# Optimization experiments

Hardware: AMD Instinct MI355X
Metric: run time of the kernel (lower is better)

The kernel has to match this reference:

```python
import jax, jax.numpy as jnp
import numpy as np

H = 128
V = 50000
B = 128
T_C = 50
T_I = 32
T_Q = 32
EPISODES = 3


def gru_cell(x, h, Wih, Whh, bih, bhh):
    # torch GRUCell math
    gi = x @ Wih.T + bih
    gh = h @ Whh.T + bhh
    ir, iz, inn = jnp.split(gi, 3, axis=-1)
    hr, hz, hn = jnp.split(gh, 3, axis=-1)
    r = jax.nn.sigmoid(ir + hr)
    z = jax.nn.sigmoid(iz + hz)
    n = jnp.tanh(inn + r * hn)
    return (1.0 - z) * n + z * h


def gru_outputs(x, Wih, Whh, bih, bhh):
    # x: (N, T, H) -> hidden at every step, (N, T, H)
    h0 = jnp.zeros((x.shape[0], x.shape[2]), x.dtype)
    def step(h, xt):
        h2 = gru_cell(xt, h, Wih, Whh, bih, bhh)
        return h2, h2
    _, ys = jax.lax.scan(step, h0, jnp.swapaxes(x, 0, 1))
    return jnp.swapaxes(ys, 0, 1)


def setup_inputs():
    key = jax.random.key(0)
    ks = iter(jax.random.split(key, 48))
    s = 0.05
    def mat(shape):
        return (jax.random.normal(next(ks), shape) * s).astype(jnp.float32)
    def gru_p(in_dim):
        return mat((3 * H, in_dim)), mat((3 * H, H)), mat((3 * H,)), mat((3 * H,))
    embed = mat((V, H)).at[0].set(0.0)  # padding_idx=0
    ig_Wih, ig_Whh, ig_bih, ig_bhh = gru_p(H)
    qg_Wih, qg_Whh, qg_bih, qg_bhh = gru_p(H)
    at_Wih, at_Whh, at_bih, at_bhh = gru_p(H)
    me_Wih, me_Whh, me_bih, me_bhh = gru_p(H)
    an_Wih, an_Whh, an_bih, an_bhh = gru_p(2 * H)
    gate_W1 = mat((H, 4 * H)); gate_b1 = mat((H,))
    gate_W2 = mat((1, H)); gate_b2 = mat((1,))
    fc_W = mat((V, H)); fc_b = jnp.zeros((V,), jnp.float32)
    facts = jax.random.randint(next(ks), (B, T_C, T_I), 0, V)
    fact_masks = jnp.zeros((B, T_C, T_I), jnp.int32)  # 0 == real token
    questions = jax.random.randint(next(ks), (B, T_Q), 0, V)
    question_masks = jnp.zeros((B, T_Q), jnp.int32)
    return dict(facts=facts, fact_masks=fact_masks, questions=questions,
                question_masks=question_masks, num_decode=8, embed=embed,
                ig_Wih=ig_Wih, ig_Whh=ig_Whh, ig_bih=ig_bih, ig_bhh=ig_bhh,
                qg_Wih=qg_Wih, qg_Whh=qg_Whh, qg_bih=qg_bih, qg_bhh=qg_bhh,
                at_Wih=at_Wih, at_Whh=at_Whh, at_bih=at_bih, at_bhh=at_bhh,
                me_Wih=me_Wih, me_Whh=me_Whh, me_bih=me_bih, me_bhh=me_bhh,
                an_Wih=an_Wih, an_Whh=an_Whh, an_bih=an_bih, an_bhh=an_bhh,
                gate_W1=gate_W1, gate_b1=gate_b1, gate_W2=gate_W2, gate_b2=gate_b2,
                fc_W=fc_W, fc_b=fc_b)


def reference(facts, fact_masks, questions, question_masks, num_decode, embed,
              ig_Wih, ig_Whh, ig_bih, ig_bhh,
              qg_Wih, qg_Whh, qg_bih, qg_bhh,
              at_Wih, at_Whh, at_bih, at_bhh,
              me_Wih, me_Whh, me_bih, me_bhh,
              an_Wih, an_Whh, an_bih, an_bhh,
              gate_W1, gate_b1, gate_W2, gate_b2, fc_W, fc_b):
    Bv, Tc, Ti = facts.shape
    Hd = embed.shape[1]

    # ---- fact encoding: one batched GRU over all B*T_C facts ----
    f = facts.reshape(Bv * Tc, Ti)
    emb = embed[f]                                            # (B*Tc, Ti, H)
    outs = gru_outputs(emb, ig_Wih, ig_Whh, ig_bih, ig_bhh)
    flen = jnp.sum(fact_masks.reshape(Bv * Tc, Ti) == 0, axis=-1)
    enc_f = jnp.take_along_axis(outs, (flen - 1)[:, None, None], axis=1)[:, 0]
    enc_f = enc_f.reshape(Bv, Tc, Hd)                         # (B, T_C, H)

    # ---- question encoding ----
    qouts = gru_outputs(embed[questions], qg_Wih, qg_Whh, qg_bih, qg_bhh)
    qlen = jnp.sum(question_masks == 0, axis=-1)
    q = jnp.take_along_axis(qouts, (qlen - 1)[:, None, None], axis=1)[:, 0]  # (B, H)

    # ---- episodic memory ----
    memory = q
    facts_t = jnp.swapaxes(enc_f, 0, 1)                       # (T_C, B, H)
    for _ in range(EPISODES):
        m = memory
        def ep_step(h, ft):
            z = jnp.concatenate([ft * q, ft * m, jnp.abs(ft - q), jnp.abs(ft - m)], axis=-1)
            g = jax.nn.sigmoid(jnp.tanh(z @ gate_W1.T + gate_b1) @ gate_W2.T + gate_b2)  # (B,1)
            h2 = gru_cell(ft, h, at_Wih, at_Whh, at_bih, at_bhh)
            return g * h2 + (1.0 - g) * h, None
        e, _ = jax.lax.scan(ep_step, jnp.zeros_like(memory), facts_t)
        memory = gru_cell(e, memory, me_Wih, me_Whh, me_bih, me_bhh)

    # ---- answer decoding (y_{t-1} stays the <s> embedding, as in the source) ----
    y0 = jnp.broadcast_to(embed[2], (Bv, Hd))                 # <s> token id = 2
    yq = jnp.concatenate([y0, q], axis=-1)                    # (B, 2H)
    def dec_step(h, _):
        h2 = gru_cell(yq, h, an_Wih, an_Whh, an_bih, an_bhh)
        return h2, jax.nn.log_softmax(h2 @ fc_W.T + fc_b, axis=-1)
    _, dec = jax.lax.scan(dec_step, memory, None, length=num_decode)  # (T, B, V)
    return jnp.swapaxes(dec, 0, 1).reshape(Bv * num_decode, -1)
```

## Files before the change

### kernel.cpp

```cpp
#include <hip/hip_runtime.h>
#include <math.h>

#define H   128
#define H3  384
#define TC  50
#define TI  32
#define TQ  32
#define NB  128
#define NF  (NB*TC)
#define EPISODES 3

typedef short  bf16x8 __attribute__((ext_vector_type(8)));
typedef short  bf16x4 __attribute__((ext_vector_type(4)));
typedef float  f32x4  __attribute__((ext_vector_type(4)));

__device__ __forceinline__ float dot4(float4 a, float4 b) {
  return a.x*b.x + a.y*b.y + a.z*b.z + a.w*b.w;
}
__device__ __forceinline__ float sigm(float x) { return 1.f/(1.f + __expf(-x)); }
__device__ __forceinline__ float tanh_f(float x) { return 1.f - 2.f/(1.f + __expf(2.f*x)); }
__device__ __forceinline__ float gru_comb(float ir, float iz, float inn,
                                          float hr, float hz, float hn, float h) {
  float r = sigm(ir + hr);
  float z = sigm(iz + hz);
  float n = tanh_f(inn + r*hn);
  return (1.f - z)*n + z*h;
}
__device__ __forceinline__ short f2bf(float x) {
  union { float f; unsigned u; } v; v.f = x;
  unsigned r = v.u + 0x7fffu + ((v.u >> 16) & 1u);
  return (short)(r >> 16);
}
__device__ __forceinline__ float bf2f(short s) {
  union { unsigned u; float f; } v; v.u = ((unsigned)(unsigned short)s) << 16;
  return v.f;
}
__device__ __forceinline__ bf16x8 pack8(float4 lo, float4 hi) {
  bf16x8 o;
  o[0]=f2bf(lo.x); o[1]=f2bf(lo.y); o[2]=f2bf(lo.z); o[3]=f2bf(lo.w);
  o[4]=f2bf(hi.x); o[5]=f2bf(hi.y); o[6]=f2bf(hi.z); o[7]=f2bf(hi.w);
  return o;
}

__global__ __launch_bounds__(256) void k_cvtall(
    const float* __restrict__ emb, short* __restrict__ emb16,
    const float* __restrict__ fcw, short* __restrict__ fcw16,
    const float* __restrict__ w0, const float* __restrict__ w1,
    const float* __restrict__ w2, short* __restrict__ w16, int VH)
{
  int bid = blockIdx.x;
  const float* src; short* dst; int n, b0, nb;
  if (bid < 1280)      { src = emb; dst = emb16; n = VH; b0 = 0;    nb = 1280; }
  else if (bid < 2560) { src = fcw; dst = fcw16; n = VH; b0 = 1280; nb = 1280; }
  else {
    int j = (bid - 2560) / 24;
    src = (j == 0) ? w0 : ((j == 1) ? w1 : w2);
    dst = w16 + (size_t)j*H3*H;
    n = H3*H; b0 = 2560 + j*24; nb = 24;
  }
  int stride = nb*256*8;
  for (int i = ((bid - b0)*256 + threadIdx.x)*8; i < n; i += stride) {
    float4 lo = *(const float4*)(src + i);
    float4 hi = *(const float4*)(src + i + 4);
    *(bf16x8*)(dst + i) = pack8(lo, hi);
  }
}

__global__ __launch_bounds__(256) void k_gather16(const short* __restrict__ emb16,
    const int* __restrict__ toks, short* __restrict__ dst)
{
  int b0 = blockIdx.x * 8;
  int r = threadIdx.x >> 5, cc = (threadIdx.x & 31)*4;
  int t = toks[b0 + r];
  *(bf16x4*)(dst + (size_t)(b0 + r)*H + cc) = *(const bf16x4*)(emb16 + (size_t)t*H + cc);
}

__global__ __launch_bounds__(256) void k_mgemmX(const short* __restrict__ A16,
    const float* __restrict__ A32, const short* __restrict__ B16,
    const float* __restrict__ bias, short* __restrict__ C, int M, int N)
{
  __shared__ __align__(16) short As[64][136];
  __shared__ __align__(16) short Bs[128][136];
  int tid = threadIdx.x;
  int lane = tid & 63, wave = tid >> 6;
  int bm = blockIdx.x, bn = blockIdx.y;
  if (A16) {
    #pragma unroll
    for (int i = 0; i < 4; ++i) {
      int ch = tid + i*256;
      int r = ch >> 4, e = (ch & 15)*8;
      int gr = bm*64 + r; if (gr > M-1) gr = M-1;
      *(bf16x8*)&As[r][e] = *(const bf16x8*)(A16 + (size_t)gr*H + e);
    }
  } else {
    #pragma unroll
    for (int i = 0; i < 4; ++i) {
      int ch = tid + i*256;
      int r = ch >> 4, e = (ch & 15)*8;
      int gr = bm*64 + r; if (gr > M-1) gr = M-1;
      const float* src = A32 + (size_t)gr*H + e;
      *(bf16x8*)&As[r][e] = pack8(*(const float4*)src, *(const float4*)(src+4));
    }
  }
  #pragma unroll
  for (int i = 0; i < 8; ++i) {
    int ch = tid + i*256;
    int r = ch >> 4, e = (ch & 15)*8;
    int gn = bn*128 + r; if (gn > N-1) gn = N-1;
    *(bf16x8*)&Bs[r][e] = *(const bf16x8*)(B16 + (size_t)gn*H + e);
  }
  __syncthreads();
  int q = lane >> 4, l15 = lane & 15;
  f32x4 acc[8];
  #pragma unroll
  for (int nt = 0; nt < 8; ++nt) { acc[nt][0]=0.f; acc[nt][1]=0.f; acc[nt][2]=0.f; acc[nt][3]=0.f; }
  int mrow = wave*16 + l15;
  #pragma unroll
  for (int kf = 0; kf < 4; ++kf) {
    bf16x8 a = *(bf16x8*)&As[mrow][q*8 + kf*32];
    #pragma unroll
    for (int nt = 0; nt < 8; ++nt) {
      bf16x8 b = *(bf16x8*)&Bs[nt*16 + l15][q*8 + kf*32];
      acc[nt] = __builtin_amdgcn_mfma_f32_16x16x32_bf16(a, b, acc[nt], 0, 0, 0);
    }
  }
  __syncthreads();
  #pragma unroll
  for (int nt = 0; nt < 8; ++nt) {
    int col = nt*16 + l15;
    float bv = bias[bn*128 + col];
    #pragma unroll
    for (int reg = 0; reg < 4; ++reg)
      Bs[wave*16 + q*4 + reg][col] = f2bf(acc[nt][reg] + bv);
  }
  __syncthreads();
  #pragma unroll
  for (int i = 0; i < 4; ++i) {
    int idx = tid + i*256;
    int r = idx >> 4, e = (idx & 15)*8;
    int gr = bm*64 + r;
    if (gr < M) *(bf16x8*)(C + (size_t)gr*N + bn*128 + e) = *(bf16x8*)&Bs[r][e];
  }
}

#define GI_STR 392
__global__ __launch_bounds__(512) void k_recgru2(
    const short* __restrict__ GI, const int* __restrict__ masks,
    const float* __restrict__ Whh, const float* __restrict__ bhh,
    float* __restrict__ enc_out, float* __restrict__ mem_out, int steps)
{
  __shared__ __align__(16) short hsb[2][16][136];
  __shared__ __align__(16) short gib[2][16][GI_STR];
  __shared__ int enc_step_s[16];
  int tid = threadIdx.x;
  int lane = tid & 63, wave = tid >> 6;
  int q = lane >> 4, l15 = lane & 15;
  int seq0 = blockIdx.x * 16;

  for (int i = tid; i < 2*16*136; i += 512) ((short*)hsb)[i] = 0;
  if (tid < 16) {
    int fl = 0;
    for (int i = 0; i < steps; ++i) fl += (masks[(size_t)(seq0+tid)*steps + i] == 0);
    int et = fl - 1; if (et < 0) et = 0; if (et >= steps) et = steps-1;
    enc_step_s[tid] = et;
  }
  bf16x8 wfrag[3][4];
  #pragma unroll
  for (int i = 0; i < 3; ++i) {
    int n = 16*wave + 128*i + l15;
    const float* wr = Whh + (size_t)n*H + q*8;
    #pragma unroll
    for (int kf = 0; kf < 4; ++kf)
      wfrag[i][kf] = pack8(*(const float4*)(wr + kf*32), *(const float4*)(wr + kf*32 + 4));
  }
  int c = 16*wave + l15;
  float bh0 = bhh[c], bh1 = bhh[c+H], bh2 = bhh[c+2*H];
  int ch0 = tid, ch1 = tid + 512;
  int r0 = ch0/48, o0 = ch0 - r0*48;
  int r1 = ch1/48, o1 = ch1 - r1*48;
  __syncthreads();
  int es[4];
  #pragma unroll
  for (int reg = 0; reg < 4; ++reg) es[reg] = enc_step_s[q*4 + reg];

  {
    size_t row0 = (size_t)(seq0 + r0)*steps;
    *(bf16x8*)&gib[0][r0][o0*8] = *((const bf16x8*)(GI + row0*H3) + o0);
    if (tid < 256) {
      size_t row1 = (size_t)(seq0 + r1)*steps;
      *(bf16x8*)&gib[0][r1][o1*8] = *((const bf16x8*)(GI + row1*H3) + o1);
    }
  }
  __syncthreads();

  float hreg[4] = {0.f, 0.f, 0.f, 0.f};
  for (int t = 0; t < steps; ++t) {
    bf16x8 pf0, pf1;
    bool havepf = (t + 1 < steps);
    if (havepf) {
      size_t row0 = (size_t)(seq0 + r0)*steps + t + 1;
      pf0 = *((const bf16x8*)(GI + row0*H3) + o0);
      if (tid < 256) {
        size_t row1 = (size_t)(seq0 + r1)*steps + t + 1;
        pf1 = *((const bf16x8*)(GI + row1*H3) + o1);
      }
    }
    f32x4 acc[3];
    #pragma unroll
    for (int i = 0; i < 3; ++i) { acc[i][0]=0.f; acc[i][1]=0.f; acc[i][2]=0.f; acc[i][3]=0.f; }
    #pragma unroll
    for (int kf = 0; kf < 4; ++kf) {
      bf16x8 a = *(bf16x8*)&hsb[t & 1][l15][kf*32 + q*8];
      #pragma unroll
      for (int i = 0; i < 3; ++i)
        acc[i] = __builtin_amdgcn_mfma_f32_16x16x32_bf16(a, wfrag[i][kf], acc[i], 0, 0, 0);
    }
    #pragma unroll
    for (int reg = 0; reg < 4; ++reg) {
      int row = q*4 + reg;
      float gr = bf2f(gib[t & 1][row][c]);
      float gz = bf2f(gib[t & 1][row][c + 128]);
      float gn = bf2f(gib[t & 1][row][c + 256]);
      float hnew = gru_comb(gr, gz, gn,
                            acc[0][reg] + bh0, acc[1][reg] + bh1, acc[2][reg] + bh2,
                            hreg[reg]);
      hreg[reg] = hnew;
      hsb[(t + 1) & 1][row][c] = f2bf(hnew);
      if (t == es[reg]) {
        enc_out[(size_t)(seq0 + row)*H + c] = hnew;
        if (mem_out) mem_out[(size_t)(seq0 + row)*H + c] = hnew;
      }
    }
    if (havepf) {
      *(bf16x8*)&gib[(t + 1) & 1][r0][o0*8] = pf0;
      if (tid < 256) *(bf16x8*)&gib[(t + 1) & 1][r1][o1*8] = pf1;
    }
    __syncthreads();
  }
}

__global__ __launch_bounds__(512) void k_facts(
    const short* __restrict__ EMB16, const short* __restrict__ WI,
    const int* __restrict__ toks, const int* __restrict__ masks,
    const float* __restrict__ Whh, const float* __restrict__ bih,
    const float* __restrict__ bhh, float* __restrict__ enc_out, int steps)
{
  __shared__ __align__(16) short hsb[2][32][136];
  __shared__ __align__(16) short esb[2][32][136];
  __shared__ int ltoks[25*TI];
  __shared__ int enc_step_s[25];
  int tid = threadIdx.x;
  int lane = tid & 63, wave = tid >> 6;
  int q = lane >> 4, l15 = lane & 15;
  int seq0 = blockIdx.x * 25;

  for (int i = tid; i < 2*32*136; i += 512) { ((short*)hsb)[i] = 0; ((short*)esb)[i] = 0; }
  for (int i = tid; i < 25*steps; i += 512)
    ltoks[i] = toks[(size_t)seq0*steps + i];
  if (tid < 25) {
    int fl = 0;
    for (int i = 0; i < steps; ++i) fl += (masks[(size_t)(seq0+tid)*steps + i] == 0);
    int et = fl - 1; if (et < 0) et = 0; if (et >= steps) et = steps-1;
    enc_step_s[tid] = et;
  }
  bf16x8 wI[3][4], wH[3][4];
  #pragma unroll
  for (int i = 0; i < 3; ++i) {
    int n = 16*wave + 128*i + l15;
    #pragma unroll
    for (int kf = 0; kf < 4; ++kf) {
      wI[i][kf] = *(const bf16x8*)(WI + (size_t)n*H + kf*32 + q*8);
      const float* wr = Whh + (size_t)n*H + kf*32 + q*8;
      wH[i][kf] = pack8(*(const float4*)wr, *(const float4*)(wr + 4));
    }
  }
  int c = 16*wave + l15;
  float bi0 = bih[c], bi1 = bih[c+H], bi2 = bih[c+2*H];
  float bh0 = bhh[c], bh1 = bhh[c+H], bh2 = bhh[c+2*H];
  int er = tid >> 4, eo = tid & 15;
  bool act = er < 25;
  __syncthreads();
  int es0[4], es1[4];
  #pragma unroll
  for (int reg = 0; reg < 4; ++reg) {
    es0[reg] = enc_step_s[q*4 + reg];
    int row2 = 16 + q*4 + reg;
    es1[reg] = (row2 < 25) ? enc_step_s[row2] : -9;
  }
  if (act) {
    int tk = ltoks[er*steps];
    *(bf16x8*)&esb[0][er][eo*8] = *((const bf16x8*)(EMB16 + (size_t)tk*H) + eo);
  }
  __syncthreads();

  float h0[4] = {0.f,0.f,0.f,0.f}, h1[4] = {0.f,0.f,0.f,0.f};
  for (int t = 0; t < steps; ++t) {
    int cur = t & 1, nxt = cur ^ 1;
    bf16x8 pf;
    bool havepf = (t + 1 < steps) && act;
    if (havepf) {
      int tk = ltoks[er*steps + t + 1];
      pf = *((const bf16x8*)(EMB16 + (size_t)tk*H) + eo);
    }
    f32x4 gi[3], gh[3];
    gi[0] = (f32x4){bi0,bi0,bi0,bi0};
    gi[1] = (f32x4){bi1,bi1,bi1,bi1};
    gi[2] = (f32x4){bi2,bi2,bi2,bi2};
    gh[0] = (f32x4){bh0,bh0,bh0,bh0};
    gh[1] = (f32x4){bh1,bh1,bh1,bh1};
    gh[2] = (f32x4){bh2,bh2,bh2,bh2};
    #pragma unroll
    for (int kf = 0; kf < 4; ++kf) {
      bf16x8 ae = *(bf16x8*)&esb[cur][l15][kf*32 + q*8];
      bf16x8 ah = *(bf16x8*)&hsb[cur][l15][kf*32 + q*8];
      #pragma unroll
      for (int i = 0; i < 3; ++i) {
        gi[i] = __builtin_amdgcn_mfma_f32_16x16x32_bf16(ae, wI[i][kf], gi[i], 0, 0, 0);
        gh[i] = __builtin_amdgcn_mfma_f32_16x16x32_bf16(ah, wH[i][kf], gh[i], 0, 0, 0);
      }
    }
    #pragma unroll
    for (int reg = 0; reg < 4; ++reg) {
      int row = q*4 + reg;
      float hnew = gru_comb(gi[0][reg], gi[1][reg], gi[2][reg],
                            gh[0][reg], gh[1][reg], gh[2][reg], h0[reg]);
      h0[reg] = hnew;
      hsb[nxt][row][c] = f2bf(hnew);
      if (t == es0[reg]) enc_out[(size_t)(seq0 + row)*H + c] = hnew;
    }
    gi[0] = (f32x4){bi0,bi0,bi0,bi0};
    gi[1] = (f32x4){bi1,bi1,bi1,bi1};
    gi[2] = (f32x4){bi2,bi2,bi2,bi2};
    gh[0] = (f32x4){bh0,bh0,bh0,bh0};
    gh[1] = (f32x4){bh1,bh1,bh1,bh1};
    gh[2] = (f32x4){bh2,bh2,bh2,bh2};
    #pragma unroll
    for (int kf = 0; kf < 4; ++kf) {
      bf16x8 ae = *(bf16x8*)&esb[cur][16 + l15][kf*32 + q*8];
      bf16x8 ah = *(bf16x8*)&hsb[cur][16 + l15][kf*32 + q*8];
      #pragma unroll
      for (int i = 0; i < 3; ++i) {
        gi[i] = __builtin_amdgcn_mfma_f32_16x16x32_bf16(ae, wI[i][kf], gi[i], 0, 0, 0);
        gh[i] = __builtin_amdgcn_mfma_f32_16x16x32_bf16(ah, wH[i][kf], gh[i], 0, 0, 0);
      }
    }
    #pragma unroll
    for (int reg = 0; reg < 4; ++reg) {
      int row2 = 16 + q*4 + reg;
      if (row2 < 25) {
        float hnew = gru_comb(gi[0][reg], gi[1][reg], gi[2][reg],
                              gh[0][reg], gh[1][reg], gh[2][reg], h1[reg]);
        h1[reg] = hnew;
        hsb[nxt][row2][c] = f2bf(hnew);
        if (t == es1[reg]) enc_out[(size_t)(seq0 + row2)*H + c] = hnew;
      }
    }
    if (havepf) *(bf16x8*)&esb[nxt][er][eo*8] = pf;
    __syncthreads();
  }
}

__global__ __launch_bounds__(128) void k_gatepre2(const float* __restrict__ encf,
    const float* __restrict__ qv, const float* __restrict__ W1,
    const float* __restrict__ b1, const float* __restrict__ W2,
    const float* __restrict__ b2, float* __restrict__ U1, float* __restrict__ gate)
{
  __shared__ float us[16][H], vs[16][H], hid[16][H], parts[16][8];
  int tid = threadIdx.x;
  int nt0 = blockIdx.x * 16;
  for (int i = tid; i < 16*H; i += 128) {
    int r = i >> 7, k = i & 127;
    int nt = nt0 + r, n = nt / TC;
    float f = encf[(size_t)nt*H + k];
    float q = qv[(size_t)n*H + k];
    us[r][k] = f*q;
    vs[r][k] = fabsf(f - q);
  }
  __syncthreads();
  int c = tid;
  float acc[16] = {};
  {
    const float* wa = W1 + (size_t)c*(4*H);
    const float* wc = wa + 2*H;
    for (int kk = 0; kk < H; kk += 16) {
      float4 a0 = *(const float4*)(wa + kk);
      float4 a1 = *(const float4*)(wa + kk + 4);
      float4 a2 = *(const float4*)(wa + kk + 8);
      float4 a3 = *(const float4*)(wa + kk + 12);
      float4 c0 = *(const float4*)(wc + kk);
      float4 c1 = *(const float4*)(wc + kk + 4);
      float4 c2 = *(const float4*)(wc + kk + 8);
      float4 c3 = *(const float4*)(wc + kk + 12);
      #pragma unroll
      for (int r = 0; r < 16; ++r) {
        const float* up = &us[r][kk];
        const float* vp = &vs[r][kk];
        acc[r] += dot4(*(const float4*)up,     a0) + dot4(*(const float4*)(up+4), a1)
                + dot4(*(const float4*)(up+8), a2) + dot4(*(const float4*)(up+12),a3)
                + dot4(*(const float4*)vp,     c0) + dot4(*(const float4*)(vp+4), c1)
                + dot4(*(const float4*)(vp+8), c2) + dot4(*(const float4*)(vp+12),c3);
      }
    }
  }
  float accm[16] = {};
  {
    const float* wb = W1 + (size_t)c*(4*H) + H;
    const float* wd = W1 + (size_t)c*(4*H) + 3*H;
    for (int kk = 0; kk < H; kk += 16) {
      float4 a0 = *(const float4*)(wb + kk);
      float4 a1 = *(const float4*)(wb + kk + 4);
      float4 a2 = *(const float4*)(wb + kk + 8);
      float4 a3 = *(const float4*)(wb + kk + 12);
      float4 c0 = *(const float4*)(wd + kk);
      float4 c1 = *(const float4*)(wd + kk + 4);
      float4 c2 = *(const float4*)(wd + kk + 8);
      float4 c3 = *(const float4*)(wd + kk + 12);
      #pragma unroll
      for (int r = 0; r < 16; ++r) {
        const float* up = &us[r][kk];
        const float* vp = &vs[r][kk];
        accm[r] += dot4(*(const float4*)up,     a0) + dot4(*(const float4*)(up+4), a1)
                 + dot4(*(const float4*)(up+8), a2) + dot4(*(const float4*)(up+12),a3)
                 + dot4(*(const float4*)vp,     c0) + dot4(*(const float4*)(vp+4), c1)
                 + dot4(*(const float4*)(vp+8), c2) + dot4(*(const float4*)(vp+12),c3);
      }
    }
  }
  float bb = b1[c];
  #pragma unroll
  for (int r = 0; r < 16; ++r) {
    float u = acc[r] + bb;
    U1[(size_t)(nt0 + r)*H + c] = u;
    hid[r][c] = tanh_f(u + accm[r]);
  }
  __syncthreads();
  {
    int r = tid >> 3, i = tid & 7;
    float p = 0.f;
    for (int k = i*16; k < i*16 + 16; ++k) p += hid[r][k]*W2[k];
    parts[r][i] = p;
  }
  __syncthreads();
  if (tid < 16) {
    float s = b2[0];
    #pragma unroll
    for (int i = 0; i < 8; ++i) s += parts[tid][i];
    gate[nt0 + tid] = sigm(s);
  }
}

__global__ __launch_bounds__(128) void k_gate(const float* __restrict__ encf,
    const float* __restrict__ mem, const float* __restrict__ W1,
    const float* __restrict__ W2, const float* __restrict__ b2,
    const float* __restrict__ U1, float* __restrict__ gate)
{
  __shared__ float us[16][H], vs[16][H], hid[16][H], parts[16][8];
  int tid = threadIdx.x;
  int nt0 = blockIdx.x * 16;
  for (int i = tid; i < 16*H; i += 128) {
    int r = i >> 7, k = i & 127;
    int nt = nt0 + r, n = nt / TC;
    float f = encf[(size_t)nt*H + k];
    float m = mem[(size_t)n*H + k];
    us[r][k] = f*m;
    vs[r][k] = fabsf(f - m);
  }
  __syncthreads();
  int c = tid;
  float acc[16];
  #pragma unroll
  for (int r = 0; r < 16; ++r) acc[r] = U1[(size_t)(nt0 + r)*H + c];
  const float* wb = W1 + (size_t)c*(4*H) + H;
  const float* wd = W1 + (size_t)c*(4*H) + 3*H;
  for (int kk = 0; kk < H; kk += 16) {
    float4 a0 = *(const float4*)(wb + kk);
    float4 a1 = *(const float4*)(wb + kk + 4);
    float4 a2 = *(const float4*)(wb + kk + 8);
    float4 a3 = *(const float4*)(wb + kk + 12);
    float4 c0 = *(const float4*)(wd + kk);
    float4 c1 = *(const float4*)(wd + kk + 4);
    float4 c2 = *(const float4*)(wd + kk + 8);
    float4 c3 = *(const float4*)(wd + kk + 12);
    #pragma unroll
    for (int r = 0; r < 16; ++r) {
      const float* up = &us[r][kk];
      const float* vp = &vs[r][kk];
      acc[r] += dot4(*(const float4*)up,     a0) + dot4(*(const float4*)(up+4), a1)
              + dot4(*(const float4*)(up+8), a2) + dot4(*(const float4*)(up+12),a3)
              + dot4(*(const float4*)vp,     c0) + dot4(*(const float4*)(vp+4), c1)
              + dot4(*(const float4*)(vp+8), c2) + dot4(*(const float4*)(vp+12),c3);
    }
  }
  #pragma unroll
  for (int r = 0; r < 16; ++r) hid[r][c] = tanh_f(acc[r]);
  __syncthreads();
  {
    int r = tid >> 3, i = tid & 7;
    float p = 0.f;
    for (int k = i*16; k < i*16 + 16; ++k) p += hid[r][k]*W2[k];
    parts[r][i] = p;
  }
  __syncthreads();
  if (tid < 16) {
    float s = b2[0];
    #pragma unroll
    for (int i = 0; i < 8; ++i) s += parts[tid][i];
    gate[nt0 + tid] = sigm(s);
  }
}

__global__ __launch_bounds__(512) void k_episode2(
    const short* __restrict__ GIat, const float* __restrict__ gate,
    const float* __restrict__ at_Whh, const float* __restrict__ at_bhh,
    const float* __restrict__ me_Wih, const float* __restrict__ me_Whh,
    const float* __restrict__ me_bih, const float* __restrict__ me_bhh,
    float* __restrict__ mem)
{
  __shared__ __align__(16) short hsb[2][16][136];
  __shared__ __align__(16) short msb[16][136];
  __shared__ __align__(16) short gib[2][16][GI_STR];
  int tid = threadIdx.x;
  int lane = tid & 63, wave = tid >> 6;
  int q = lane >> 4, l15 = lane & 15;
  int n0 = blockIdx.x * 16;

  for (int i = tid; i < 2*16*136; i += 512) ((short*)hsb)[i] = 0;
  for (int i = tid; i < 16*H; i += 512) {
    int r = i >> 7, cc = i & 127;
    msb[r][cc] = f2bf(mem[(size_t)(n0 + r)*H + cc]);
  }
  bf16x8 wfrag[3][4];
  #pragma unroll
  for (int i = 0; i < 3; ++i) {
    int n = 16*wave + 128*i + l15;
    const float* wr = at_Whh + (size_t)n*H + q*8;
    #pragma unroll
    for (int kf = 0; kf < 4; ++kf)
      wfrag[i][kf] = pack8(*(const float4*)(wr + kf*32), *(const float4*)(wr + kf*32 + 4));
  }
  int c = 16*wave + l15;
  float bh0 = at_bhh[c], bh1 = at_bhh[c+H], bh2 = at_bhh[c+2*H];
  int ch0 = tid, ch1 = tid + 512;
  int r0 = ch0/48, o0 = ch0 - r0*48;
  int r1 = ch1/48, o1 = ch1 - r1*48;
  __syncthreads();

  *(bf16x8*)&gib[0][r0][o0*8] = *((const bf16x8*)(GIat + (size_t)(n0 + r0)*TC*H3) + o0);
  if (tid < 256)
    *(bf16x8*)&gib[0][r1][o1*8] = *((const bf16x8*)(GIat + (size_t)(n0 + r1)*TC*H3) + o1);
  __syncthreads();

  float hreg[4] = {0.f, 0.f, 0.f, 0.f};
  for (int t = 0; t < TC; ++t) {
    bf16x8 pf0, pf1;
    bool havepf = (t + 1 < TC);
    if (havepf) {
      pf0 = *((const bf16x8*)(GIat + ((size_t)(n0 + r0)*TC + t + 1)*H3) + o0);
      if (tid < 256)
        pf1 = *((const bf16x8*)(GIat + ((size_t)(n0 + r1)*TC + t + 1)*H3) + o1);
    }
    f32x4 acc[3];
    #pragma unroll
    for (int i = 0; i < 3; ++i) { acc[i][0]=0.f; acc[i][1]=0.f; acc[i][2]=0.f; acc[i][3]=0.f; }
    #pragma unroll
    for (int kf = 0; kf < 4; ++kf) {
      bf16x8 a = *(bf16x8*)&hsb[t & 1][l15][kf*32 + q*8];
      #pragma unroll
      for (int i = 0; i < 3; ++i)
        acc[i] = __builtin_amdgcn_mfma_f32_16x16x32_bf16(a, wfrag[i][kf], acc[i], 0, 0, 0);
    }
    #pragma unroll
    for (int reg = 0; reg < 4; ++reg) {
      int row = q*4 + reg;
      float g  = gate[(size_t)(n0 + row)*TC + t];
      float gr = bf2f(gib[t & 1][row][c]);
      float gz = bf2f(gib[t & 1][row][c + 128]);
      float gn = bf2f(gib[t & 1][row][c + 256]);
      float h2 = gru_comb(gr, gz, gn,
                          acc[0][reg] + bh0, acc[1][reg] + bh1, acc[2][reg] + bh2,
                          hreg[reg]);
      float hnew = g*h2 + (1.f - g)*hreg[reg];
      hreg[reg] = hnew;
      hsb[(t + 1) & 1][row][c] = f2bf(hnew);
    }
    if (havepf) {
      *(bf16x8*)&gib[(t + 1) & 1][r0][o0*8] = pf0;
      if (tid < 256) *(bf16x8*)&gib[(t + 1) & 1][r1][o1*8] = pf1;
    }
    __syncthreads();
  }
  f32x4 gi_acc[3], gh_acc[3];
  #pragma unroll
  for (int i = 0; i < 3; ++i) {
    gi_acc[i][0]=0.f; gi_acc[i][1]=0.f; gi_acc[i][2]=0.f; gi_acc[i][3]=0.f;
    gh_acc[i][0]=0.f; gh_acc[i][1]=0.f; gh_acc[i][2]=0.f; gh_acc[i][3]=0.f;
  }
  #pragma unroll
  for (int i = 0; i < 3; ++i) {
    int n = 16*wave + 128*i + l15;
    const float* wr = me_Wih + (size_t)n*H + q*8;
    #pragma unroll
    for (int kf = 0; kf < 4; ++kf)
      wfrag[i][kf] = pack8(*(const float4*)(wr + kf*32), *(const float4*)(wr + kf*32 + 4));
  }
  #pragma unroll
  for (int kf = 0; kf < 4; ++kf) {
    bf16x8 a = *(bf16x8*)&hsb[TC & 1][l15][kf*32 + q*8];
    #pragma unroll
    for (int i = 0; i < 3; ++i)
      gi_acc[i] = __builtin_amdgcn_mfma_f32_16x16x32_bf16(a, wfrag[i][kf], gi_acc[i], 0, 0, 0);
  }
  #pragma unroll
  for (int i = 0; i < 3; ++i) {
    int n = 16*wave + 128*i + l15;
    const float* wr = me_Whh + (size_t)n*H + q*8;
    #pragma unroll
    for (int kf = 0; kf < 4; ++kf)
      wfrag[i][kf] = pack8(*(const float4*)(wr + kf*32), *(const float4*)(wr + kf*32 + 4));
  }
  #pragma unroll
  for (int kf = 0; kf < 4; ++kf) {
    bf16x8 a = *(bf16x8*)&msb[l15][kf*32 + q*8];
    #pragma unroll
    for (int i = 0; i < 3; ++i)
      gh_acc[i] = __builtin_amdgcn_mfma_f32_16x16x32_bf16(a, wfrag[i][kf], gh_acc[i], 0, 0, 0);
  }
  float bi0 = me_bih[c], bi1 = me_bih[c+H], bi2 = me_bih[c+2*H];
  float bo0 = me_bhh[c], bo1 = me_bhh[c+H], bo2 = me_bhh[c+2*H];
  #pragma unroll
  for (int reg = 0; reg < 4; ++reg) {
    int row = q*4 + reg;
    float m = mem[(size_t)(n0 + row)*H + c];
    float mnew = gru_comb(gi_acc[0][reg] + bi0, gi_acc[1][reg] + bi1, gi_acc[2][reg] + bi2,
                          gh_acc[0][reg] + bo0, gh_acc[1][reg] + bo1, gh_acc[2][reg] + bo2, m);
    mem[(size_t)(n0 + row)*H + c] = mnew;
  }
}

__global__ __launch_bounds__(384) void k_decode(const float* __restrict__ embed,
    const float* __restrict__ qv, const float* __restrict__ mem,
    const float* __restrict__ an_Wih, const float* __restrict__ an_Whh,
    const float* __restrict__ an_bih, const float* __restrict__ an_bhh,
    short* __restrict__ h2d16, int ND)
{
  __shared__ float hs[2][H], qs[2][H], e2[H], ghs[2][H3], gis[2][H3];
  int tid = threadIdx.x;
  int n0 = blockIdx.x * 2;
  if (tid < H) e2[tid] = embed[2*H + tid];
  if (tid < 256) {
    int r = tid >> 7, c = tid & 127;
    hs[r][c] = mem[(size_t)(n0 + r)*H + c];
    qs[r][c] = qv[(size_t)(n0 + r)*H + c];
  }
  __syncthreads();
  {
    const float* wp = an_Wih + (size_t)tid*(2*H);
    float se = 0.f, sq0 = 0.f, sq1 = 0.f;
    for (int kk = 0; kk < H; kk += 16) {
      float4 w0 = *(const float4*)(wp + kk);
      float4 w1 = *(const float4*)(wp + kk + 4);
      float4 w2 = *(const float4*)(wp + kk + 8);
      float4 w3 = *(const float4*)(wp + kk + 12);
      const float* ep = &e2[kk];
      se += dot4(*(const float4*)ep,     w0) + dot4(*(const float4*)(ep+4), w1)
          + dot4(*(const float4*)(ep+8), w2) + dot4(*(const float4*)(ep+12),w3);
      float4 u0 = *(const float4*)(wp + H + kk);
      float4 u1 = *(const float4*)(wp + H + kk + 4);
      float4 u2 = *(const float4*)(wp + H + kk + 8);
      float4 u3 = *(const float4*)(wp + H + kk + 12);
      const float* q0 = &qs[0][kk];
      const float* q1 = &qs[1][kk];
      sq0 += dot4(*(const float4*)q0,     u0) + dot4(*(const float4*)(q0+4), u1)
           + dot4(*(const float4*)(q0+8), u2) + dot4(*(const float4*)(q0+12),u3);
      sq1 += dot4(*(const float4*)q1,     u0) + dot4(*(const float4*)(q1+4), u1)
           + dot4(*(const float4*)(q1+8), u2) + dot4(*(const float4*)(q1+12),u3);
    }
    float b = an_bih[tid];
    gis[0][tid] = b + se + sq0;
    gis[1][tid] = b + se + sq1;
  }
  const float* whp = an_Whh + (size_t)tid*H;
  float bh = an_bhh[tid];
  for (int t = 0; t < ND; ++t) {
    float a0 = 0.f, a1 = 0.f;
    for (int kk = 0; kk < H; kk += 16) {
      float4 w0 = *(const float4*)(whp + kk);
      float4 w1 = *(const float4*)(whp + kk + 4);
      float4 w2 = *(const float4*)(whp + kk + 8);
      float4 w3 = *(const float4*)(whp + kk + 12);
      const float* h0p = &hs[0][kk];
      const float* h1p = &hs[1][kk];
      a0 += dot4(*(const float4*)h0p,     w0) + dot4(*(const float4*)(h0p+4), w1)
          + dot4(*(const float4*)(h0p+8), w2) + dot4(*(const float4*)(h0p+12),w3);
      a1 += dot4(*(const float4*)h1p,     w0) + dot4(*(const float4*)(h1p+4), w1)
          + dot4(*(const float4*)(h1p+8), w2) + dot4(*(const float4*)(h1p+12),w3);
    }
    ghs[0][tid] = a0 + bh;
    ghs[1][tid] = a1 + bh;
    __syncthreads();
    if (tid < 256) {
      int r = tid >> 7, c = tid & 127;
      float h2 = gru_comb(gis[r][c], gis[r][c+H], gis[r][c+2*H],
                          ghs[r][c], ghs[r][c+H], ghs[r][c+2*H], hs[r][c]);
      hs[r][c] = h2;
      h2d16[((size_t)(n0 + r)*ND + t)*H + c] = f2bf(h2);
    }
    __syncthreads();
  }
}

__global__ __launch_bounds__(256) void k_lpass1p(const short* __restrict__ A16,
    const short* __restrict__ B16, const float* __restrict__ bias,
    float2* __restrict__ partials, int M, int N, int NSL)
{
  __shared__ __align__(16) short As[64][136];
  __shared__ __align__(16) short Bs[128][136];
  int tid = threadIdx.x;
  int lane = tid & 63, wave = tid >> 6;
  int q = lane >> 4, l15 = lane & 15;
  int bn = blockIdx.x;
  #pragma unroll
  for (int i = 0; i < 8; ++i) {
    int ch = tid + i*256;
    int r = ch >> 4, e = (ch & 15)*8;
    int gn = bn*128 + r; if (gn > N-1) gn = N-1;
    *(bf16x8*)&Bs[r][e] = *(const bf16x8*)(B16 + (size_t)gn*H + e);
  }
  float bv[8];
  #pragma unroll
  for (int nt = 0; nt < 8; ++nt) {
    int col = bn*128 + nt*16 + l15;
    bv[nt] = (col < N) ? bias[col] : 0.f;
  }
  int mrow = wave*16 + l15;
  for (int rt = 0; rt < 16; ++rt) {
    __syncthreads();
    #pragma unroll
    for (int i = 0; i < 4; ++i) {
      int ch = tid + i*256;
      int r = ch >> 4, e = (ch & 15)*8;
      *(bf16x8*)&As[r][e] = *(const bf16x8*)(A16 + (size_t)(rt*64 + r)*H + e);
    }
    __syncthreads();
    f32x4 acc[8];
    #pragma unroll
    for (int nt = 0; nt < 8; ++nt) { acc[nt][0]=0.f; acc[nt][1]=0.f; acc[nt][2]=0.f; acc[nt][3]=0.f; }
    #pragma unroll
    for (int kf = 0; kf < 4; ++kf) {
      bf16x8 a = *(bf16x8*)&As[mrow][q*8 + kf*32];
      #pragma unroll
      for (int nt = 0; nt < 8; ++nt) {
        bf16x8 b = *(bf16x8*)&Bs[nt*16 + l15][q*8 + kf*32];
        acc[nt] = __builtin_amdgcn_mfma_f32_16x16x32_bf16(a, b, acc[nt], 0, 0, 0);
      }
    }
    #pragma unroll
    for (int reg = 0; reg < 4; ++reg) {
      float xs[8], cm = -3.4e38f;
      #pragma unroll
      for (int nt = 0; nt < 8; ++nt) {
        int col = bn*128 + nt*16 + l15;
        float x = (col < N) ? (acc[nt][reg] + bv[nt]) : -3.4e38f;
        xs[nt] = x; cm = fmaxf(cm, x);
      }
      #pragma unroll
      for (int off = 1; off < 16; off <<= 1) cm = fmaxf(cm, __shfl_xor(cm, off));
      float ss = 0.f;
      #pragma unroll
      for (int nt = 0; nt < 8; ++nt) ss += __expf(xs[nt] - cm);
      #pragma unroll
      for (int off = 1; off < 16; off <<= 1) ss += __shfl_xor(ss, off);
      if (l15 == 0) {
        int row = rt*64 + wave*16 + q*4 + reg;
        partials[(size_t)row*NSL + bn] = make_float2(cm, ss);
      }
    }
  }
}

__global__ __launch_bounds__(256) void k_lse2(const float2* __restrict__ partials,
                                              float* __restrict__ lse, int M, int NSL)
{
  int wave = threadIdx.x >> 6, lane = threadIdx.x & 63;
  int row = blockIdx.x*4 + wave;
  if (row >= M) return;
  float m = -3.4e38f, s = 0.f;
  for (int i = lane; i < NSL; i += 64) {
    float2 p = partials[(size_t)row*NSL + i];
    float nm = fmaxf(m, p.x);
    s = s*__expf(m - nm) + p.y*__expf(p.x - nm);
    m = nm;
  }
  #pragma unroll
  for (int off = 32; off; off >>= 1) {
    float mo = __shfl_xor(m, off);
    float so = __shfl_xor(s, off);
    float nm = fmaxf(m, mo);
    s = s*__expf(m - nm) + so*__expf(mo - nm);
    m = nm;
  }
  if (lane == 0) lse[row] = m + logf(s);
}

__global__ __launch_bounds__(256) void k_lpass2p(const short* __restrict__ A16,
    const short* __restrict__ B16, const float* __restrict__ bias,
    const float* __restrict__ lse, float* __restrict__ C, int M, int N, int NT)
{
  __shared__ __align__(16) short As[64][136];
  __shared__ __align__(16) short Bs[128][136];
  __shared__ float lss[960];
  int tid = threadIdx.x;
  int lane = tid & 63, wave = tid >> 6;
  int q = lane >> 4, l15 = lane & 15;
  int bn = blockIdx.x;
  #pragma unroll
  for (int i = 0; i < 8; ++i) {
    int ch = tid + i*256;
    int r = ch >> 4, e = (ch & 15)*8;
    int gn = bn*128 + r; if (gn > N-1) gn = N-1;
    *(bf16x8*)&Bs[r][e] = *(const bf16x8*)(B16 + (size_t)gn*H + e);
  }
  for (int i = tid; i < NT*64; i += 256) lss[i] = lse[i];
  float bv[8];
  #pragma unroll
  for (int nt = 0; nt < 8; ++nt) {
    int col = bn*128 + nt*16 + l15;
    bv[nt] = (col < N) ? bias[col] : 0.f;
  }
  int mrow = wave*16 + l15;
  for (int rt = 0; rt < NT; ++rt) {
    __syncthreads();
    #pragma unroll
    for (int i = 0; i < 4; ++i) {
      int ch = tid + i*256;
      int r = ch >> 4, e = (ch & 15)*8;
      *(bf16x8*)&As[r][e] = *(const bf16x8*)(A16 + (size_t)(rt*64 + r)*H + e);
    }
    __syncthreads();
    f32x4 acc[8];
    #pragma unroll
    for (int nt = 0; nt < 8; ++nt) { acc[nt][0]=0.f; acc[nt][1]=0.f; acc[nt][2]=0.f; acc[nt][3]=0.f; }
    #pragma unroll
    for (int kf = 0; kf < 4; ++kf) {
      bf16x8 a = *(bf16x8*)&As[mrow][q*8 + kf*32];
      #pragma unroll
      for (int nt = 0; nt < 8; ++nt) {
        bf16x8 b = *(bf16x8*)&Bs[nt*16 + l15][q*8 + kf*32];
        acc[nt] = __builtin_amdgcn_mfma_f32_16x16x32_bf16(a, b, acc[nt], 0, 0, 0);
      }
    }
    #pragma unroll
    for (int nt = 0; nt < 8; ++nt) {
      int gcol = bn*128 + nt*16 + l15;
      if (gcol < N) {
        #pragma unroll
        for (int reg = 0; reg < 4; ++reg) {
          int row = rt*64 + wave*16 + q*4 + reg;
          C[(size_t)row*N + gcol] = acc[nt][reg] + bv[nt] - lss[row];
        }
      }
    }
  }
}

__global__ __launch_bounds__(256) void k_lpass2(const short* __restrict__ A16,
    const short* __restrict__ B16, const float* __restrict__ B32,
    const float* __restrict__ bias, const float* __restrict__ lse,
    float* __restrict__ C, int M, int N, int bm_off)
{
  __shared__ __align__(16) short As[64][136];
  __shared__ __align__(16) short Bs[128][136];
  int tid = threadIdx.x;
  int lane = tid & 63, wave = tid >> 6;
  int q = lane >> 4, l15 = lane & 15;
  int bm = blockIdx.x + bm_off, bn = blockIdx.y;
  #pragma unroll
  for (int i = 0; i < 4; ++i) {
    int ch = tid + i*256;
    int r = ch >> 4, e = (ch & 15)*8;
    int gr = bm*64 + r; if (gr > M-1) gr = M-1;
    *(bf16x8*)&As[r][e] = *(const bf16x8*)(A16 + (size_t)gr*H + e);
  }
  if (B16) {
    #pragma unroll
    for (int i = 0; i < 8; ++i) {
      int ch = tid + i*256;
      int r = ch >> 4, e = (ch & 15)*8;
      int gn = bn*128 + r; if (gn > N-1) gn = N-1;
      *(bf16x8*)&Bs[r][e] = *(const bf16x8*)(B16 + (size_t)gn*H + e);
    }
  } else {
    #pragma unroll
    for (int i = 0; i < 8; ++i) {
      int ch = tid + i*256;
      int r = ch >> 4, e = (ch & 15)*8;
      int gn = bn*128 + r; if (gn > N-1) gn = N-1;
      const float* src = B32 + (size_t)gn*H + e;
      *(bf16x8*)&Bs[r][e] = pack8(*(const float4*)src, *(const float4*)(src+4));
    }
  }
  __syncthreads();
  f32x4 acc[8];
  #pragma unroll
  for (int nt = 0; nt < 8; ++nt) { acc[nt][0]=0.f; acc[nt][1]=0.f; acc[nt][2]=0.f; acc[nt][3]=0.f; }
  int mrow = wave*16 + l15;
  #pragma unroll
  for (int kf = 0; kf < 4; ++kf) {
    bf16x8 a = *(bf16x8*)&As[mrow][q*8 + kf*32];
    #pragma unroll
    for (int nt = 0; nt < 8; ++nt) {
      bf16x8 b = *(bf16x8*)&Bs[nt*16 + l15][q*8 + kf*32];
      acc[nt] = __builtin_amdgcn_mfma_f32_16x16x32_bf16(a, b, acc[nt], 0, 0, 0);
    }
  }
  __syncthreads();
  float (*Cs)[132] = (float(*)[132])&Bs[0][0];
  float lrow[4];
  #pragma unroll
  for (int reg = 0; reg < 4; ++reg) {
    int row = bm*64 + wave*16 + q*4 + reg;
    lrow[reg] = lse[row < M ? row : M-1];
  }
  #pragma unroll
  for (int nt = 0; nt < 8; ++nt) {
    int col = nt*16 + l15;
    int gcol = bn*128 + col;
    float bv = (gcol < N) ? bias[gcol] : 0.f;
    #pragma unroll
    for (int reg = 0; reg < 4; ++reg)
      Cs[wave*16 + q*4 + reg][col] = acc[nt][reg] + bv - lrow[reg];
  }
  __syncthreads();
  #pragma unroll
  for (int i = 0; i < 8; ++i) {
    int idx = tid + i*256;
    int r = idx >> 5, c4 = (idx & 31)*4;
    int gr = bm*64 + r;
    int gc = bn*128 + c4;
    if (gr < M && gc + 3 < N)
      *(float4*)(C + (size_t)gr*N + gc) = *(float4*)&Cs[r][c4];
    else if (gr < M) {
      #pragma unroll
      for (int j = 0; j < 4; ++j)
        if (gc + j < N) C[(size_t)gr*N + gc + j] = Cs[r][c4 + j];
    }
  }
}

extern "C" void kernel_launch(void* const* d_in, const int* in_sizes, int n_in,
                              void* d_out, int out_size, void* d_ws, size_t ws_size,
                              hipStream_t stream) {
  const int*   facts     = (const int*)  d_in[0];
  const int*   fmask     = (const int*)  d_in[1];
  const int*   questions = (const int*)  d_in[2];
  const int*   qmask     = (const int*)  d_in[3];
  const float* embed     = (const float*)d_in[5];
  const float* ig_Wih    = (const float*)d_in[6];
  const float* ig_Whh    = (const float*)d_in[7];
  const float* ig_bih    = (const float*)d_in[8];
  const float* ig_bhh    = (const float*)d_in[9];
  const float* qg_Wih    = (const float*)d_in[10];
  const float* qg_Whh    = (const float*)d_in[11];
  const float* qg_bih    = (const float*)d_in[12];
  const float* qg_bhh    = (const float*)d_in[13];
  const float* at_Wih    = (const float*)d_in[14];
  const float* at_Whh    = (const float*)d_in[15];
  const float* at_bih    = (const float*)d_in[16];
  const float* at_bhh    = (const float*)d_in[17];
  const float* me_Wih    = (const float*)d_in[18];
  const float* me_Whh    = (const float*)d_in[19];
  const float* me_bih    = (const float*)d_in[20];
  const float* me_bhh    = (const float*)d_in[21];
  const float* an_Wih    = (const float*)d_in[22];
  const float* an_Whh    = (const float*)d_in[23];
  const float* an_bih    = (const float*)d_in[24];
  const float* an_bhh    = (const float*)d_in[25];
  const float* gate_W1   = (const float*)d_in[26];
  const float* gate_b1   = (const float*)d_in[27];
  const float* gate_W2   = (const float*)d_in[28];
  const float* gate_b2   = (const float*)d_in[29];
  const float* fc_W      = (const float*)d_in[30];
  const float* fc_b      = (const float*)d_in[31];
  (void)n_in; (void)ws_size;

  const int V   = in_sizes[5] / H;
  const int ND  = out_size / (NB * V);
  const int M   = NB * ND;
  const int NSL = (V + 127) / 128;

  float* OUT = (float*)d_out;
  size_t oPART  = 0;
  size_t oEMB16 = oPART + (size_t)M*NSL*2;
  size_t oEMBQ  = oEMB16 + (size_t)V*64;
  size_t oQGI   = oEMBQ + (size_t)NB*TQ*64;
  size_t oGIAT  = oQGI  + (size_t)NB*TQ*192;
  size_t oU1    = oGIAT + (size_t)NF*192;
  size_t oGATE  = oU1   + (size_t)NF*H;
  size_t oW16   = oGATE + NF;
  float2* partials = (float2*)(OUT + oPART);
  short* EMB16  = (short*)(OUT + oEMB16);
  short* EMBQ16 = (short*)(OUT + oEMBQ);
  short* QGIsh  = (short*)(OUT + oQGI);
  short* GIATsh = (short*)(OUT + oGIAT);
  float* U1b    = OUT + oU1;
  float* GATE   = OUT + oGATE;
  short* igW16  = (short*)(OUT + oW16);
  short* qgW16  = igW16 + (size_t)H3*H;
  short* atW16  = qgW16 + (size_t)H3*H;
  short* FCW16  = (short*)(OUT + (size_t)(M - 64)*V);

  float* encf  = (float*)d_ws;
  float* qvec  = encf + (size_t)NF*H;
  float* mem   = qvec + (size_t)NB*H;
  short* H2D16 = (short*)(mem + (size_t)NB*H);
  float* lse   = (float*)(H2D16 + (size_t)M*H);

  k_cvtall<<<2632, 256, 0, stream>>>(embed, EMB16, fc_W, FCW16,
                                     ig_Wih, qg_Wih, at_Wih, igW16, V*H);
  k_gather16<<<NB*TQ/8, 256, 0, stream>>>(EMB16, questions, EMBQ16);
  k_mgemmX<<<dim3(NB*TQ/64, H3/128), 256, 0, stream>>>(EMBQ16, nullptr, qgW16, qg_bih, QGIsh, NB*TQ, H3);
  k_facts<<<NF/25, 512, 0, stream>>>(EMB16, igW16, facts, fmask, ig_Whh, ig_bih, ig_bhh, encf, TI);
  k_recgru2<<<NB/16, 512, 0, stream>>>(QGIsh, qmask, qg_Whh, qg_bhh, qvec, mem, TQ);
  k_mgemmX<<<dim3(NF/64, H3/128), 256, 0, stream>>>(nullptr, encf, atW16, at_bih, GIATsh, NF, H3);
  k_gatepre2<<<NF/16, 128, 0, stream>>>(encf, qvec, gate_W1, gate_b1, gate_W2, gate_b2, U1b, GATE);
  k_episode2<<<NB/16, 512, 0, stream>>>(GIATsh, GATE, at_Whh, at_bhh,
                                        me_Wih, me_Whh, me_bih, me_bhh, mem);
  for (int e = 1; e < EPISODES; ++e) {
    k_gate<<<NF/16, 128, 0, stream>>>(encf, mem, gate_W1, gate_W2, gate_b2, U1b, GATE);
    k_episode2<<<NB/16, 512, 0, stream>>>(GIATsh, GATE, at_Whh, at_bhh,
                                          me_Wih, me_Whh, me_bih, me_bhh, mem);
  }
  k_decode<<<NB/2, 384, 0, stream>>>(embed, qvec, mem, an_Wih, an_Whh, an_bih, an_bhh,
                                     H2D16, ND);
  k_lpass1p<<<NSL, 256, 0, stream>>>(H2D16, FCW16, fc_b, partials, M, V, NSL);
  k_lse2<<<(M+3)/4, 256, 0, stream>>>(partials, lse, M, NSL);
  k_lpass2p<<<NSL, 256, 0, stream>>>(H2D16, FCW16, fc_b, lse, OUT, M, V, (M/64) - 1);
  k_lpass2<<<dim3(1, NSL), 256, 0, stream>>>(H2D16, nullptr, fc_W, fc_b, lse,
                                             OUT, M, V, (M/64) - 1);
}
```

Baseline: 956.7 us.

## Fuse question gather, facts/question GRUs, GIAT gemm with gate, coalesce logits stores

```diff
diff --git a/kernel.cpp b/kernel.cpp
--- a/kernel.cpp
+++ b/kernel.cpp
@@ -66,17 +66,8 @@
   }
 }
 
-__global__ __launch_bounds__(256) void k_gather16(const short* __restrict__ emb16,
-    const int* __restrict__ toks, short* __restrict__ dst)
-{
-  int b0 = blockIdx.x * 8;
-  int r = threadIdx.x >> 5, cc = (threadIdx.x & 31)*4;
-  int t = toks[b0 + r];
-  *(bf16x4*)(dst + (size_t)(b0 + r)*H + cc) = *(const bf16x4*)(emb16 + (size_t)t*H + cc);
-}
-
 __global__ __launch_bounds__(256) void k_mgemmX(const short* __restrict__ A16,
-    const float* __restrict__ A32, const short* __restrict__ B16,
+    const int* __restrict__ toks, const short* __restrict__ B16,
     const float* __restrict__ bias, short* __restrict__ C, int M, int N)
 {
   __shared__ __align__(16) short As[64][136];
@@ -84,23 +75,13 @@
   int tid = threadIdx.x;
   int lane = tid & 63, wave = tid >> 6;
   int bm = blockIdx.x, bn = blockIdx.y;
-  if (A16) {
-    #pragma unroll
-    for (int i = 0; i < 4; ++i) {
-      int ch = tid + i*256;
-      int r = ch >> 4, e = (ch & 15)*8;
-      int gr = bm*64 + r; if (gr > M-1) gr = M-1;
-      *(bf16x8*)&As[r][e] = *(const bf16x8*)(A16 + (size_t)gr*H + e);
-    }
-  } else {
-    #pragma unroll
-    for (int i = 0; i < 4; ++i) {
-      int ch = tid + i*256;
-      int r = ch >> 4, e = (ch & 15)*8;
-      int gr = bm*64 + r; if (gr > M-1) gr = M-1;
-      const float* src = A32 + (size_t)gr*H + e;
-      *(bf16x8*)&As[r][e] = pack8(*(const float4*)src, *(const float4*)(src+4));
-    }
+  #pragma unroll
+  for (int i = 0; i < 4; ++i) {
+    int ch = tid + i*256;
+    int r = ch >> 4, e = (ch & 15)*8;
+    int gr = bm*64 + r; if (gr > M-1) gr = M-1;
+    size_t arow = toks ? (size_t)toks[gr] : (size_t)gr;
+    *(bf16x8*)&As[r][e] = *(const bf16x8*)(A16 + arow*H + e);
   }
   #pragma unroll
   for (int i = 0; i < 8; ++i) {
@@ -144,320 +125,388 @@
 }
 
 #define GI_STR 392
-__global__ __launch_bounds__(512) void k_recgru2(
-    const short* __restrict__ GI, const int* __restrict__ masks,
-    const float* __restrict__ Whh, const float* __restrict__ bhh,
-    float* __restrict__ enc_out, float* __restrict__ mem_out, int steps)
+__global__ __launch_bounds__(512) void k_factsq(
+    const short* __restrict__ EMB16, const short* __restrict__ WI,
+    const int* __restrict__ toks, const int* __restrict__ masks,
+    const float* __restrict__ Whh, const float* __restrict__ bih,
+    const float* __restrict__ bhh, float* __restrict__ enc_out,
+    const short* __restrict__ QGI, const int* __restrict__ qmasks,
+    const float* __restrict__ qWhh, const float* __restrict__ qbhh,
+    float* __restrict__ qvec, float* __restrict__ mem_out)
 {
-  __shared__ __align__(16) short hsb[2][16][136];
-  __shared__ __align__(16) short gib[2][16][GI_STR];
-  __shared__ int enc_step_s[16];
+  __shared__ __align__(16) char smem[38464];
   int tid = threadIdx.x;
   int lane = tid & 63, wave = tid >> 6;
   int q = lane >> 4, l15 = lane & 15;
-  int seq0 = blockIdx.x * 16;
-
-  for (int i = tid; i < 2*16*136; i += 512) ((short*)hsb)[i] = 0;
-  if (tid < 16) {
-    int fl = 0;
-    for (int i = 0; i < steps; ++i) fl += (masks[(size_t)(seq0+tid)*steps + i] == 0);
-    int et = fl - 1; if (et < 0) et = 0; if (et >= steps) et = steps-1;
-    enc_step_s[tid] = et;
-  }
-  bf16x8 wfrag[3][4];
-  #pragma unroll
-  for (int i = 0; i < 3; ++i) {
-    int n = 16*wave + 128*i + l15;
-    const float* wr = Whh + (size_t)n*H + q*8;
-    #pragma unroll
-    for (int kf = 0; kf < 4; ++kf)
-      wfrag[i][kf] = pack8(*(const float4*)(wr + kf*32), *(const float4*)(wr + kf*32 + 4));
-  }
-  int c = 16*wave + l15;
-  float bh0 = bhh[c], bh1 = bhh[c+H], bh2 = bhh[c+2*H];
-  int ch0 = tid, ch1 = tid + 512;
-  int r0 = ch0/48, o0 = ch0 - r0*48;
-  int r1 = ch1/48, o1 = ch1 - r1*48;
-  __syncthreads();
-  int es[4];
-  #pragma unroll
-  for (int reg = 0; reg < 4; ++reg) es[reg] = enc_step_s[q*4 + reg];
-
-  {
-    size_t row0 = (size_t)(seq0 + r0)*steps;
-    *(bf16x8*)&gib[0][r0][o0*8] = *((const bf16x8*)(GI + row0*H3) + o0);
-    if (tid < 256) {
-      size_t row1 = (size_t)(seq0 + r1)*steps;
-      *(bf16x8*)&gib[0][r1][o1*8] = *((const bf16x8*)(GI + row1*H3) + o1);
-    }
-  }
-  __syncthreads();
-
-  float hreg[4] = {0.f, 0.f, 0.f, 0.f};
-  for (int t = 0; t < steps; ++t) {
-    bf16x8 pf0, pf1;
-    bool havepf = (t + 1 < steps);
-    if (havepf) {
-      size_t row0 = (size_t)(seq0 + r0)*steps + t + 1;
-      pf0 = *((const bf16x8*)(GI + row0*H3) + o0);
+
+  if (blockIdx.x < 256) {
+    short (*hsb)[136] = (short(*)[136])smem;
+    short (*esb)[136] = (short(*)[136])(smem + 17408);
+    int* ltoks = (int*)(smem + 34816);
+    int* enc_step_s = (int*)(smem + 38016);
+    int seq0 = blockIdx.x * 25;
+    const int steps = TI;
+
+    {
+      short* p0 = (short*)smem;
+      short* p1 = (short*)(smem + 17408);
+      for (int i = tid; i < 2*32*136; i += 512) { p0[i] = 0; p1[i] = 0; }
+    }
+    for (int i = tid; i < 25*steps; i += 512)
+      ltoks[i] = toks[(size_t)seq0*steps + i];
+    if (tid < 25) {
+      int fl = 0;
+      for (int i = 0; i < steps; ++i) fl += (masks[(size_t)(seq0+tid)*steps + i] == 0);
+      int et = fl - 1; if (et < 0) et = 0; if (et >= steps) et = steps-1;
+      enc_step_s[tid] = et;
+    }
+    bf16x8 wI[3][4], wH[3][4];
+    #pragma unroll
+    for (int i = 0; i < 3; ++i) {
+      int n = 16*wave + 128*i + l15;
+      #pragma unroll
+      for (int kf = 0; kf < 4; ++kf) {
+        wI[i][kf] = *(const bf16x8*)(WI + (size_t)n*H + kf*32 + q*8);
+        const float* wr = Whh + (size_t)n*H + kf*32 + q*8;
+        wH[i][kf] = pack8(*(const float4*)wr, *(const float4*)(wr + 4));
+      }
+    }
+    int c = 16*wave + l15;
+    float bi0 = bih[c], bi1 = bih[c+H], bi2 = bih[c+2*H];
+    float bh0 = bhh[c], bh1 = bhh[c+H], bh2 = bhh[c+2*H];
+    int er = tid >> 4, eo = tid & 15;
+    bool act = er < 25;
+    __syncthreads();
+    int es0[4], es1[4];
+    #pragma unroll
+    for (int reg = 0; reg < 4; ++reg) {
+      es0[reg] = enc_step_s[q*4 + reg];
+      int row2 = 16 + q*4 + reg;
+      es1[reg] = (row2 < 25) ? enc_step_s[row2] : -9;
+    }
+    if (act) {
+      int tk = ltoks[er*steps];
+      *(bf16x8*)&esb[er][eo*8] = *((const bf16x8*)(EMB16 + (size_t)tk*H) + eo);
+    }
+    __syncthreads();
+
+    float h0[4] = {0.f,0.f,0.f,0.f}, h1[4] = {0.f,0.f,0.f,0.f};
+    for (int t = 0; t < steps; ++t) {
+      int cur = (t & 1)*32, nxt = ((t+1) & 1)*32;
+      bf16x8 pf;
+      bool havepf = (t + 1 < steps) && act;
+      if (havepf) {
+        int tk = ltoks[er*steps + t + 1];
+        pf = *((const bf16x8*)(EMB16 + (size_t)tk*H) + eo);
+      }
+      f32x4 gi[3], gh[3];
+      gi[0] = (f32x4){bi0,bi0,bi0,bi0};
+      gi[1] = (f32x4){bi1,bi1,bi1,bi1};
+      gi[2] = (f32x4){bi2,bi2,bi2,bi2};
+      gh[0] = (f32x4){bh0,bh0,bh0,bh0};
+      gh[1] = (f32x4){bh1,bh1,bh1,bh1};
+      gh[2] = (f32x4){bh2,bh2,bh2,bh2};
+      #pragma unroll
+      for (int kf = 0; kf < 4; ++kf) {
+        bf16x8 ae = *(bf16x8*)&esb[cur + l15][kf*32 + q*8];
+        bf16x8 ah = *(bf16x8*)&hsb[cur + l15][kf*32 + q*8];
+        #pragma unroll
+        for (int i = 0; i < 3; ++i) {
+          gi[i] = __builtin_amdgcn_mfma_f32_16x16x32_bf16(ae, wI[i][kf], gi[i], 0, 0, 0);
+          gh[i] = __builtin_amdgcn_mfma_f32_16x16x32_bf16(ah, wH[i][kf], gh[i], 0, 0, 0);
+        }
+      }
+      #pragma unroll
+      for (int reg = 0; reg < 4; ++reg) {
+        int row = q*4 + reg;
+        float hnew = gru_comb(gi[0][reg], gi[1][reg], gi[2][reg],
+                              gh[0][reg], gh[1][reg], gh[2][reg], h0[reg]);
+        h0[reg] = hnew;
+        hsb[nxt + row][c] = f2bf(hnew);
+        if (t == es0[reg]) enc_out[(size_t)(seq0 + row)*H + c] = hnew;
+      }
+      gi[0] = (f32x4){bi0,bi0,bi0,bi0};
+      gi[1] = (f32x4){bi1,bi1,bi1,bi1};
+      gi[2] = (f32x4){bi2,bi2,bi2,bi2};
+      gh[0] = (f32x4){bh0,bh0,bh0,bh0};
+      gh[1] = (f32x4){bh1,bh1,bh1,bh1};
+      gh[2] = (f32x4){bh2,bh2,bh2,bh2};
+      #pragma unroll
+      for (int kf = 0; kf < 4; ++kf) {
+        bf16x8 ae = *(bf16x8*)&esb[cur + 16 + l15][kf*32 + q*8];
+        bf16x8 ah = *(bf16x8*)&hsb[cur + 16 + l15][kf*32 + q*8];
+        #pragma unroll
+        for (int i = 0; i < 3; ++i) {
+          gi[i] = __builtin_amdgcn_mfma_f32_16x16x32_bf16(ae, wI[i][kf], gi[i], 0, 0, 0);
+          gh[i] = __builtin_amdgcn_mfma_f32_16x16x32_bf16(ah, wH[i][kf], gh[i], 0, 0, 0);
+        }
+      }
+      #pragma unroll
+      for (int reg = 0; reg < 4; ++reg) {
+        int row2 = 16 + q*4 + reg;
+        if (row2 < 25) {
+          float hnew = gru_comb(gi[0][reg], gi[1][reg], gi[2][reg],
+                                gh[0][reg], gh[1][reg], gh[2][reg], h1[reg]);
+          h1[reg] = hnew;
+          hsb[nxt + row2][c] = f2bf(hnew);
+          if (t == es1[reg]) enc_out[(size_t)(seq0 + row2)*H + c] = hnew;
+        }
+      }
+      if (havepf) *(bf16x8*)&esb[nxt + er][eo*8] = pf;
+      __syncthreads();
+    }
+  } else {
+    short (*hsb)[136] = (short(*)[136])smem;
+    short (*gib)[GI_STR] = (short(*)[GI_STR])(smem + 8704);
+    int* enc_step_s = (int*)(smem + 33792);
+    int seq0 = (blockIdx.x - 256) * 16;
+    const int steps = TQ;
+
+    {
+      short* p0 = (short*)smem;
+      for (int i = tid; i < 2*16*136; i += 512) p0[i] = 0;
+    }
+    if (tid < 16) {
+      int fl = 0;
+      for (int i = 0; i < steps; ++i) fl += (qmasks[(size_t)(seq0+tid)*steps + i] == 0);
+      int et = fl - 1; if (et < 0) et = 0; if (et >= steps) et = steps-1;
+      enc_step_s[tid] = et;
+    }
+    bf16x8 wfrag[3][4];
+    #pragma unroll
+    for (int i = 0; i < 3; ++i) {
+      int n = 16*wave + 128*i + l15;
+      const float* wr = qWhh + (size_t)n*H + q*8;
+      #pragma unroll
+      for (int kf = 0; kf < 4; ++kf)
+        wfrag[i][kf] = pack8(*(const float4*)(wr + kf*32), *(const float4*)(wr + kf*32 + 4));
+    }
+    int c = 16*wave + l15;
+    float bh0 = qbhh[c], bh1 = qbhh[c+H], bh2 = qbhh[c+2*H];
+    int ch0 = tid, ch1 = tid + 512;
+    int r0 = ch0/48, o0 = ch0 - r0*48;
+    int r1 = ch1/48, o1 = ch1 - r1*48;
+    __syncthreads();
+    int es[4];
+    #pragma unroll
+    for (int reg = 0; reg < 4; ++reg) es[reg] = enc_step_s[q*4 + reg];
+
+    {
+      size_t row0 = (size_t)(seq0 + r0)*steps;
+      *(bf16x8*)&gib[r0][o0*8] = *((const bf16x8*)(QGI + row0*H3) + o0);
       if (tid < 256) {
-        size_t row1 = (size_t)(seq0 + r1)*steps + t + 1;
-        pf1 = *((const bf16x8*)(GI + row1*H3) + o1);
-      }
-    }
-    f32x4 acc[3];
-    #pragma unroll
-    for (int i = 0; i < 3; ++i) { acc[i][0]=0.f; acc[i][1]=0.f; acc[i][2]=0.f; acc[i][3]=0.f; }
-    #pragma unroll
-    for (int kf = 0; kf < 4; ++kf) {
-      bf16x8 a = *(bf16x8*)&hsb[t & 1][l15][kf*32 + q*8];
-      #pragma unroll
-      for (int i = 0; i < 3; ++i)
-        acc[i] = __builtin_amdgcn_mfma_f32_16x16x32_bf16(a, wfrag[i][kf], acc[i], 0, 0, 0);
-    }
-    #pragma unroll
-    for (int reg = 0; reg < 4; ++reg) {
-      int row = q*4 + reg;
-      float gr = bf2f(gib[t & 1][row][c]);
-      float gz = bf2f(gib[t & 1][row][c + 128]);
-      float gn = bf2f(gib[t & 1][row][c + 256]);
-      float hnew = gru_comb(gr, gz, gn,
-                            acc[0][reg] + bh0, acc[1][reg] + bh1, acc[2][reg] + bh2,
-                            hreg[reg]);
-      hreg[reg] = hnew;
-      hsb[(t + 1) & 1][row][c] = f2bf(hnew);
-      if (t == es[reg]) {
-        enc_out[(size_t)(seq0 + row)*H + c] = hnew;
-        if (mem_out) mem_out[(size_t)(seq0 + row)*H + c] = hnew;
-      }
-    }
-    if (havepf) {
-      *(bf16x8*)&gib[(t + 1) & 1][r0][o0*8] = pf0;
-      if (tid < 256) *(bf16x8*)&gib[(t + 1) & 1][r1][o1*8] = pf1;
-    }
-    __syncthreads();
-  }
-}
-
-__global__ __launch_bounds__(512) void k_facts(
-    const short* __restrict__ EMB16, const short* __restrict__ WI,
-    const int* __restrict__ toks, const int* __restrict__ masks,
-    const float* __restrict__ Whh, const float* __restrict__ bih,
-    const float* __restrict__ bhh, float* __restrict__ enc_out, int steps)
-{
-  __shared__ __align__(16) short hsb[2][32][136];
-  __shared__ __align__(16) short esb[2][32][136];
-  __shared__ int ltoks[25*TI];
-  __shared__ int enc_step_s[25];
-  int tid = threadIdx.x;
-  int lane = tid & 63, wave = tid >> 6;
-  int q = lane >> 4, l15 = lane & 15;
-  int seq0 = blockIdx.x * 25;
-
-  for (int i = tid; i < 2*32*136; i += 512) { ((short*)hsb)[i] = 0; ((short*)esb)[i] = 0; }
-  for (int i = tid; i < 25*steps; i += 512)
-    ltoks[i] = toks[(size_t)seq0*steps + i];
-  if (tid < 25) {
-    int fl = 0;
-    for (int i = 0; i < steps; ++i) fl += (masks[(size_t)(seq0+tid)*steps + i] == 0);
-    int et = fl - 1; if (et < 0) et = 0; if (et >= steps) et = steps-1;
-    enc_step_s[tid] = et;
-  }
-  bf16x8 wI[3][4], wH[3][4];
-  #pragma unroll
-  for (int i = 0; i < 3; ++i) {
-    int n = 16*wave + 128*i + l15;
-    #pragma unroll
-    for (int kf = 0; kf < 4; ++kf) {
-      wI[i][kf] = *(const bf16x8*)(WI + (size_t)n*H + kf*32 + q*8);
-      const float* wr = Whh + (size_t)n*H + kf*32 + q*8;
-      wH[i][kf] = pack8(*(const float4*)wr, *(const float4*)(wr + 4));
-    }
-  }
-  int c = 16*wave + l15;
-  float bi0 = bih[c], bi1 = bih[c+H], bi2 = bih[c+2*H];
-  float bh0 = bhh[c], bh1 = bhh[c+H], bh2 = bhh[c+2*H];
-  int er = tid >> 4, eo = tid & 15;
-  bool act = er < 25;
-  __syncthreads();
-  int es0[4], es1[4];
-  #pragma unroll
-  for (int reg = 0; reg < 4; ++reg) {
-    es0[reg] = enc_step_s[q*4 + reg];
-    int row2 = 16 + q*4 + reg;
-    es1[reg] = (row2 < 25) ? enc_step_s[row2] : -9;
-  }
-  if (act) {
-    int tk = ltoks[er*steps];
-    *(bf16x8*)&esb[0][er][eo*8] = *((const bf16x8*)(EMB16 + (size_t)tk*H) + eo);
-  }
-  __syncthreads();
-
-  float h0[4] = {0.f,0.f,0.f,0.f}, h1[4] = {0.f,0.f,0.f,0.f};
-  for (int t = 0; t < steps; ++t) {
-    int cur = t & 1, nxt = cur ^ 1;
-    bf16x8 pf;
-    bool havepf = (t + 1 < steps) && act;
-    if (havepf) {
-      int tk = ltoks[er*steps + t + 1];
-      pf = *((const bf16x8*)(EMB16 + (size_t)tk*H) + eo);
-    }
-    f32x4 gi[3], gh[3];
-    gi[0] = (f32x4){bi0,bi0,bi0,bi0};
-    gi[1] = (f32x4){bi1,bi1,bi1,bi1};
-    gi[2] = (f32x4){bi2,bi2,bi2,bi2};
-    gh[0] = (f32x4){bh0,bh0,bh0,bh0};
-    gh[1] = (f32x4){bh1,bh1,bh1,bh1};
-    gh[2] = (f32x4){bh2,bh2,bh2,bh2};
-    #pragma unroll
-    for (int kf = 0; kf < 4; ++kf) {
-      bf16x8 ae = *(bf16x8*)&esb[cur][l15][kf*32 + q*8];
-      bf16x8 ah = *(bf16x8*)&hsb[cur][l15][kf*32 + q*8];
-      #pragma unroll
-      for (int i = 0; i < 3; ++i) {
-        gi[i] = __builtin_amdgcn_mfma_f32_16x16x32_bf16(ae, wI[i][kf], gi[i], 0, 0, 0);
-        gh[i] = __builtin_amdgcn_mfma_f32_16x16x32_bf16(ah, wH[i][kf], gh[i], 0, 0, 0);
-      }
-    }
-    #pragma unroll
-    for (int reg = 0; reg < 4; ++reg) {
-      int row = q*4 + reg;
-      float hnew = gru_comb(gi[0][reg], gi[1][reg], gi[2][reg],
-                            gh[0][reg], gh[1][reg], gh[2][reg], h0[reg]);
-      h0[reg] = hnew;
-      hsb[nxt][row][c] = f2bf(hnew);
-      if (t == es0[reg]) enc_out[(size_t)(seq0 + row)*H + c] = hnew;
-    }
-    gi[0] = (f32x4){bi0,bi0,bi0,bi0};
-    gi[1] = (f32x4){bi1,bi1,bi1,bi1};
-    gi[2] = (f32x4){bi2,bi2,bi2,bi2};
-    gh[0] = (f32x4){bh0,bh0,bh0,bh0};
-    gh[1] = (f32x4){bh1,bh1,bh1,bh1};
-    gh[2] = (f32x4){bh2,bh2,bh2,bh2};
-    #pragma unroll
-    for (int kf = 0; kf < 4; ++kf) {
-      bf16x8 ae = *(bf16x8*)&esb[cur][16 + l15][kf*32 + q*8];
-      bf16x8 ah = *(bf16x8*)&hsb[cur][16 + l15][kf*32 + q*8];
-      #pragma unroll
-      for (int i = 0; i < 3; ++i) {
-        gi[i] = __builtin_amdgcn_mfma_f32_16x16x32_bf16(ae, wI[i][kf], gi[i], 0, 0, 0);
-        gh[i] = __builtin_amdgcn_mfma_f32_16x16x32_bf16(ah, wH[i][kf], gh[i], 0, 0, 0);
-      }
-    }
-    #pragma unroll
-    for (int reg = 0; reg < 4; ++reg) {
-      int row2 = 16 + q*4 + reg;
-      if (row2 < 25) {
-        float hnew = gru_comb(gi[0][reg], gi[1][reg], gi[2][reg],
-                              gh[0][reg], gh[1][reg], gh[2][reg], h1[reg]);
-        h1[reg] = hnew;
-        hsb[nxt][row2][c] = f2bf(hnew);
-        if (t == es1[reg]) enc_out[(size_t)(seq0 + row2)*H + c] = hnew;
-      }
-    }
-    if (havepf) *(bf16x8*)&esb[nxt][er][eo*8] = pf;
-    __syncthreads();
-  }
-}
-
-__global__ __launch_bounds__(128) void k_gatepre2(const float* __restrict__ encf,
+        size_t row1 = (size_t)(seq0 + r1)*steps;
+        *(bf16x8*)&gib[r1][o1*8] = *((const bf16x8*)(QGI + row1*H3) + o1);
+      }
+    }
+    __syncthreads();
+
+    float hreg[4] = {0.f, 0.f, 0.f, 0.f};
+    for (int t = 0; t < steps; ++t) {
+      int cur = (t & 1)*16, nxt = ((t+1) & 1)*16;
+      bf16x8 pf0, pf1;
+      bool havepf = (t + 1 < steps);
+      if (havepf) {
+        size_t row0 = (size_t)(seq0 + r0)*steps + t + 1;
+        pf0 = *((const bf16x8*)(QGI + row0*H3) + o0);
+        if (tid < 256) {
+          size_t row1 = (size_t)(seq0 + r1)*steps + t + 1;
+          pf1 = *((const bf16x8*)(QGI + row1*H3) + o1);
+        }
+      }
+      f32x4 acc[3];
+      #pragma unroll
+      for (int i = 0; i < 3; ++i) { acc[i][0]=0.f; acc[i][1]=0.f; acc[i][2]=0.f; acc[i][3]=0.f; }
+      #pragma unroll
+      for (int kf = 0; kf < 4; ++kf) {
+        bf16x8 a = *(bf16x8*)&hsb[cur + l15][kf*32 + q*8];
+        #pragma unroll
+        for (int i = 0; i < 3; ++i)
+          acc[i] = __builtin_amdgcn_mfma_f32_16x16x32_bf16(a, wfrag[i][kf], acc[i], 0, 0, 0);
+      }
+      #pragma unroll
+      for (int reg = 0; reg < 4; ++reg) {
+        int row = q*4 + reg;
+        float gr = bf2f(gib[cur + row][c]);
+        float gz = bf2f(gib[cur + row][c + 128]);
+        float gn = bf2f(gib[cur + row][c + 256]);
+        float hnew = gru_comb(gr, gz, gn,
+                              acc[0][reg] + bh0, acc[1][reg] + bh1, acc[2][reg] + bh2,
+                              hreg[reg]);
+        hreg[reg] = hnew;
+        hsb[nxt + row][c] = f2bf(hnew);
+        if (t == es[reg]) {
+          qvec[(size_t)(seq0 + row)*H + c] = hnew;
+          mem_out[(size_t)(seq0 + row)*H + c] = hnew;
+        }
+      }
+      if (havepf) {
+        *(bf16x8*)&gib[nxt + r0][o0*8] = pf0;
+        if (tid < 256) *(bf16x8*)&gib[nxt + r1][o1*8] = pf1;
+      }
+      __syncthreads();
+    }
+  }
+}
+
+__global__ __launch_bounds__(256) void k_giat_gate0(
+    const float* __restrict__ encf, const short* __restrict__ atW16,
+    const float* __restrict__ at_bih, short* __restrict__ GIAT,
     const float* __restrict__ qv, const float* __restrict__ W1,
     const float* __restrict__ b1, const float* __restrict__ W2,
     const float* __restrict__ b2, float* __restrict__ U1, float* __restrict__ gate)
 {
-  __shared__ float us[16][H], vs[16][H], hid[16][H], parts[16][8];
+  __shared__ __align__(16) char smem[52224];
   int tid = threadIdx.x;
-  int nt0 = blockIdx.x * 16;
-  for (int i = tid; i < 16*H; i += 128) {
-    int r = i >> 7, k = i & 127;
-    int nt = nt0 + r, n = nt / TC;
-    float f = encf[(size_t)nt*H + k];
-    float q = qv[(size_t)n*H + k];
-    us[r][k] = f*q;
-    vs[r][k] = fabsf(f - q);
-  }
-  __syncthreads();
-  int c = tid;
-  float acc[16] = {};
-  {
-    const float* wa = W1 + (size_t)c*(4*H);
-    const float* wc = wa + 2*H;
-    for (int kk = 0; kk < H; kk += 16) {
-      float4 a0 = *(const float4*)(wa + kk);
-      float4 a1 = *(const float4*)(wa + kk + 4);
-      float4 a2 = *(const float4*)(wa + kk + 8);
-      float4 a3 = *(const float4*)(wa + kk + 12);
-      float4 c0 = *(const float4*)(wc + kk);
-      float4 c1 = *(const float4*)(wc + kk + 4);
-      float4 c2 = *(const float4*)(wc + kk + 8);
-      float4 c3 = *(const float4*)(wc + kk + 12);
-      #pragma unroll
-      for (int r = 0; r < 16; ++r) {
-        const float* up = &us[r][kk];
-        const float* vp = &vs[r][kk];
-        acc[r] += dot4(*(const float4*)up,     a0) + dot4(*(const float4*)(up+4), a1)
-                + dot4(*(const float4*)(up+8), a2) + dot4(*(const float4*)(up+12),a3)
-                + dot4(*(const float4*)vp,     c0) + dot4(*(const float4*)(vp+4), c1)
-                + dot4(*(const float4*)(vp+8), c2) + dot4(*(const float4*)(vp+12),c3);
-      }
-    }
-  }
-  float accm[16] = {};
-  {
-    const float* wb = W1 + (size_t)c*(4*H) + H;
-    const float* wd = W1 + (size_t)c*(4*H) + 3*H;
-    for (int kk = 0; kk < H; kk += 16) {
-      float4 a0 = *(const float4*)(wb + kk);
-      float4 a1 = *(const float4*)(wb + kk + 4);
-      float4 a2 = *(const float4*)(wb + kk + 8);
-      float4 a3 = *(const float4*)(wb + kk + 12);
-      float4 c0 = *(const float4*)(wd + kk);
-      float4 c1 = *(const float4*)(wd + kk + 4);
-      float4 c2 = *(const float4*)(wd + kk + 8);
-      float4 c3 = *(const float4*)(wd + kk + 12);
-      #pragma unroll
-      for (int r = 0; r < 16; ++r) {
-        const float* up = &us[r][kk];
-        const float* vp = &vs[r][kk];
-        accm[r] += dot4(*(const float4*)up,     a0) + dot4(*(const float4*)(up+4), a1)
-                 + dot4(*(const float4*)(up+8), a2) + dot4(*(const float4*)(up+12),a3)
-                 + dot4(*(const float4*)vp,     c0) + dot4(*(const float4*)(vp+4), c1)
-                 + dot4(*(const float4*)(vp+8), c2) + dot4(*(const float4*)(vp+12),c3);
-      }
-    }
-  }
-  float bb = b1[c];
-  #pragma unroll
-  for (int r = 0; r < 16; ++r) {
-    float u = acc[r] + bb;
-    U1[(size_t)(nt0 + r)*H + c] = u;
-    hid[r][c] = tanh_f(u + accm[r]);
-  }
-  __syncthreads();
-  {
-    int r = tid >> 3, i = tid & 7;
-    float p = 0.f;
-    for (int k = i*16; k < i*16 + 16; ++k) p += hid[r][k]*W2[k];
-    parts[r][i] = p;
-  }
-  __syncthreads();
-  if (tid < 16) {
-    float s = b2[0];
-    #pragma unroll
-    for (int i = 0; i < 8; ++i) s += parts[tid][i];
-    gate[nt0 + tid] = sigm(s);
-  }
-}
-
-__global__ __launch_bounds__(128) void k_gate(const float* __restrict__ encf,
+  if (blockIdx.x < 300) {
+    short (*As)[136] = (short(*)[136])smem;
+    short (*Bs)[136] = (short(*)[136])(smem + 17408);
+    int bm = blockIdx.x % 100, bn = blockIdx.x / 100;
+    int lane = tid & 63, wave = tid >> 6;
+    int q = lane >> 4, l15 = lane & 15;
+    #pragma unroll
+    for (int i = 0; i < 4; ++i) {
+      int ch = tid + i*256;
+      int r = ch >> 4, e = (ch & 15)*8;
+      int gr = bm*64 + r;
+      const float* src = encf + (size_t)gr*H + e;
+      *(bf16x8*)&As[r][e] = pack8(*(const float4*)src, *(const float4*)(src+4));
+    }
+    #pragma unroll
+    for (int i = 0; i < 8; ++i) {
+      int ch = tid + i*256;
+      int r = ch >> 4, e = (ch & 15)*8;
+      int gn = bn*128 + r;
+      *(bf16x8*)&Bs[r][e] = *(const bf16x8*)(atW16 + (size_t)gn*H + e);
+    }
+    __syncthreads();
+    f32x4 acc[8];
+    #pragma unroll
+    for (int nt = 0; nt < 8; ++nt) { acc[nt][0]=0.f; acc[nt][1]=0.f; acc[nt][2]=0.f; acc[nt][3]=0.f; }
+    int mrow = wave*16 + l15;
+    #pragma unroll
+    for (int kf = 0; kf < 4; ++kf) {
+      bf16x8 a = *(bf16x8*)&As[mrow][q*8 + kf*32];
+      #pragma unroll
+      for (int nt = 0; nt < 8; ++nt) {
+        bf16x8 b = *(bf16x8*)&Bs[nt*16 + l15][q*8 + kf*32];
+        acc[nt] = __builtin_amdgcn_mfma_f32_16x16x32_bf16(a, b, acc[nt], 0, 0, 0);
+      }
+    }
+    __syncthreads();
+    #pragma unroll
+    for (int nt = 0; nt < 8; ++nt) {
+      int col = nt*16 + l15;
+      float bv = at_bih[bn*128 + col];
+      #pragma unroll
+      for (int reg = 0; reg < 4; ++reg)
+        Bs[wave*16 + q*4 + reg][col] = f2bf(acc[nt][reg] + bv);
+    }
+    __syncthreads();
+    #pragma unroll
+    for (int i = 0; i < 4; ++i) {
+      int idx = tid + i*256;
+      int r = idx >> 4, e = (idx & 15)*8;
+      int gr = bm*64 + r;
+      *(bf16x8*)(GIAT + (size_t)gr*H3 + bn*128 + e) = *(bf16x8*)&Bs[r][e];
+    }
+  } else {
+    float* us = (float*)smem;
+    float* vs = us + 32*128;
+    float* hid = vs + 32*128;
+    float* parts = hid + 32*128;
+    int nt0 = (blockIdx.x - 300) * 32;
+    for (int i = tid; i < 32*128; i += 256) {
+      int r = i >> 7, k = i & 127;
+      int nt = nt0 + r, n = nt / TC;
+      float f = encf[(size_t)nt*H + k];
+      float qq = qv[(size_t)n*H + k];
+      us[i] = f*qq;
+      vs[i] = fabsf(f - qq);
+    }
+    __syncthreads();
+    int c = tid & 127, rbase = (tid >> 7)*16;
+    float acc[16] = {};
+    {
+      const float* wa = W1 + (size_t)c*(4*H);
+      const float* wc = wa + 2*H;
+      for (int kk = 0; kk < H; kk += 16) {
+        float4 a0 = *(const float4*)(wa + kk);
+        float4 a1 = *(const float4*)(wa + kk + 4);
+        float4 a2 = *(const float4*)(wa + kk + 8);
+        float4 a3 = *(const float4*)(wa + kk + 12);
+        float4 c0 = *(const float4*)(wc + kk);
+        float4 c1 = *(const float4*)(wc + kk + 4);
+        float4 c2 = *(const float4*)(wc + kk + 8);
+        float4 c3 = *(const float4*)(wc + kk + 12);
+        #pragma unroll
+        for (int r = 0; r < 16; ++r) {
+          const float* up = &us[(rbase + r)*128 + kk];
+          const float* vp = &vs[(rbase + r)*128 + kk];
+          acc[r] += dot4(*(const float4*)up,     a0) + dot4(*(const float4*)(up+4), a1)
+                  + dot4(*(const float4*)(up+8), a2) + dot4(*(const float4*)(up+12),a3)
+                  + dot4(*(const float4*)vp,     c0) + dot4(*(const float4*)(vp+4), c1)
+                  + dot4(*(const float4*)(vp+8), c2) + dot4(*(const float4*)(vp+12),c3);
+        }
+      }
+    }
+    float accm[16] = {};
+    {
+      const float* wb = W1 + (size_t)c*(4*H) + H;
+      const float* wd = W1 + (size_t)c*(4*H) + 3*H;
+      for (int kk = 0; kk < H; kk += 16) {
+        float4 a0 = *(const float4*)(wb + kk);
+        float4 a1 = *(const float4*)(wb + kk + 4);
+        float4 a2 = *(const float4*)(wb + kk + 8);
+        float4 a3 = *(const float4*)(wb + kk + 12);
+        float4 c0 = *(const float4*)(wd + kk);
+        float4 c1 = *(const float4*)(wd + kk + 4);
+        float4 c2 = *(const float4*)(wd + kk + 8);
+        float4 c3 = *(const float4*)(wd + kk + 12);
+        #pragma unroll
+        for (int r = 0; r < 16; ++r) {
+          const float* up = &us[(rbase + r)*128 + kk];
+          const float* vp = &vs[(rbase + r)*128 + kk];
+          accm[r] += dot4(*(const float4*)up,     a0) + dot4(*(const float4*)(up+4), a1)
+                   + dot4(*(const float4*)(up+8), a2) + dot4(*(const float4*)(up+12),a3)
+                   + dot4(*(const float4*)vp,     c0) + dot4(*(const float4*)(vp+4), c1)
+                   + dot4(*(const float4*)(vp+8), c2) + dot4(*(const float4*)(vp+12),c3);
+        }
+      }
+    }
+    float bb = b1[c];
+    #pragma unroll
+    for (int r = 0; r < 16; ++r) {
+      float u = acc[r] + bb;
+      U1[(size_t)(nt0 + rbase + r)*H + c] = u;
+      hid[(rbase + r)*128 + c] = tanh_f(u + accm[r]);
+    }
+    __syncthreads();
+    {
+      int r = tid >> 3, i = tid & 7;
+      float p = 0.f;
+      for (int k = i*16; k < i*16 + 16; ++k) p += hid[r*128 + k]*W2[k];
+      parts[r*8 + i] = p;
+    }
+    __syncthreads();
+    if (tid < 32) {
+      float s = b2[0];
+      #pragma unroll
+      for (int i = 0; i < 8; ++i) s += parts[tid*8 + i];
+      gate[nt0 + tid] = sigm(s);
+    }
+  }
+}
+
+__global__ __launch_bounds__(256) void k_gate256(const float* __restrict__ encf,
     const float* __restrict__ mem, const float* __restrict__ W1,
     const float* __restrict__ W2, const float* __restrict__ b2,
     const float* __restrict__ U1, float* __restrict__ gate)
 {
-  __shared__ float us[16][H], vs[16][H], hid[16][H], parts[16][8];
+  __shared__ float us[32][128], vs[32][128], hid[32][128], parts[32][8];
   int tid = threadIdx.x;
-  int nt0 = blockIdx.x * 16;
-  for (int i = tid; i < 16*H; i += 128) {
+  int nt0 = blockIdx.x * 32;
+  for (int i = tid; i < 32*128; i += 256) {
     int r = i >> 7, k = i & 127;
     int nt = nt0 + r, n = nt / TC;
     float f = encf[(size_t)nt*H + k];
@@ -466,10 +515,10 @@
     vs[r][k] = fabsf(f - m);
   }
   __syncthreads();
-  int c = tid;
+  int c = tid & 127, rbase = (tid >> 7)*16;
   float acc[16];
   #pragma unroll
-  for (int r = 0; r < 16; ++r) acc[r] = U1[(size_t)(nt0 + r)*H + c];
+  for (int r = 0; r < 16; ++r) acc[r] = U1[(size_t)(nt0 + rbase + r)*H + c];
   const float* wb = W1 + (size_t)c*(4*H) + H;
   const float* wd = W1 + (size_t)c*(4*H) + 3*H;
   for (int kk = 0; kk < H; kk += 16) {
@@ -483,8 +532,8 @@
     float4 c3 = *(const float4*)(wd + kk + 12);
     #pragma unroll
     for (int r = 0; r < 16; ++r) {
-      const float* up = &us[r][kk];
-      const float* vp = &vs[r][kk];
+      const float* up = &us[rbase + r][kk];
+      const float* vp = &vs[rbase + r][kk];
       acc[r] += dot4(*(const float4*)up,     a0) + dot4(*(const float4*)(up+4), a1)
               + dot4(*(const float4*)(up+8), a2) + dot4(*(const float4*)(up+12),a3)
               + dot4(*(const float4*)vp,     c0) + dot4(*(const float4*)(vp+4), c1)
@@ -492,7 +541,7 @@
     }
   }
   #pragma unroll
-  for (int r = 0; r < 16; ++r) hid[r][c] = tanh_f(acc[r]);
+  for (int r = 0; r < 16; ++r) hid[rbase + r][c] = tanh_f(acc[r]);
   __syncthreads();
   {
     int r = tid >> 3, i = tid & 7;
@@ -501,7 +550,7 @@
     parts[r][i] = p;
   }
   __syncthreads();
-  if (tid < 16) {
+  if (tid < 32) {
     float s = b2[0];
     #pragma unroll
     for (int i = 0; i < 8; ++i) s += parts[tid][i];
@@ -756,23 +805,17 @@
     }
     #pragma unroll
     for (int reg = 0; reg < 4; ++reg) {
-      float xs[8], cm = -3.4e38f;
+      float ss = 0.f;
       #pragma unroll
       for (int nt = 0; nt < 8; ++nt) {
         int col = bn*128 + nt*16 + l15;
-        float x = (col < N) ? (acc[nt][reg] + bv[nt]) : -3.4e38f;
-        xs[nt] = x; cm = fmaxf(cm, x);
-      }
-      #pragma unroll
-      for (int off = 1; off < 16; off <<= 1) cm = fmaxf(cm, __shfl_xor(cm, off));
-      float ss = 0.f;
-      #pragma unroll
-      for (int nt = 0; nt < 8; ++nt) ss += __expf(xs[nt] - cm);
+        if (col < N) ss += __expf(acc[nt][reg] + bv[nt]);
+      }
       #pragma unroll
       for (int off = 1; off < 16; off <<= 1) ss += __shfl_xor(ss, off);
       if (l15 == 0) {
         int row = rt*64 + wave*16 + q*4 + reg;
-        partials[(size_t)row*NSL + bn] = make_float2(cm, ss);
+        partials[(size_t)row*NSL + bn] = make_float2(0.f, ss);
       }
     }
   }
@@ -809,6 +852,7 @@
   __shared__ __align__(16) short As[64][136];
   __shared__ __align__(16) short Bs[128][136];
   __shared__ float lss[960];
+  float (*cs)[132] = (float(*)[132])&As[0][0];
   int tid = threadIdx.x;
   int lane = tid & 63, wave = tid >> 6;
   int q = lane >> 4, l15 = lane & 15;
@@ -849,24 +893,52 @@
         acc[nt] = __builtin_amdgcn_mfma_f32_16x16x32_bf16(a, b, acc[nt], 0, 0, 0);
       }
     }
-    #pragma unroll
-    for (int nt = 0; nt < 8; ++nt) {
-      int gcol = bn*128 + nt*16 + l15;
-      if (gcol < N) {
+    float lrow[4];
+    #pragma unroll
+    for (int reg = 0; reg < 4; ++reg)
+      lrow[reg] = lss[rt*64 + wave*16 + q*4 + reg];
+    __syncthreads();
+    if (wave < 2) {
+      #pragma unroll
+      for (int nt = 0; nt < 8; ++nt)
         #pragma unroll
-        for (int reg = 0; reg < 4; ++reg) {
-          int row = rt*64 + wave*16 + q*4 + reg;
-          C[(size_t)row*N + gcol] = acc[nt][reg] + bv[nt] - lss[row];
-        }
-      }
+        for (int reg = 0; reg < 4; ++reg)
+          cs[wave*16 + q*4 + reg][nt*16 + l15] = acc[nt][reg] + bv[nt] - lrow[reg];
+    }
+    __syncthreads();
+    #pragma unroll
+    for (int j = 0; j < 4; ++j) {
+      int idx = tid + j*256;
+      int r = idx >> 5, c4 = (idx & 31)*4;
+      int gr = rt*64 + r;
+      int gc = bn*128 + c4;
+      if (gc + 3 < N) *(float4*)(C + (size_t)gr*N + gc) = *(float4*)&cs[r][c4];
+      else { for (int e = 0; e < 4; ++e) if (gc + e < N) C[(size_t)gr*N + gc + e] = cs[r][c4 + e]; }
+    }
+    __syncthreads();
+    if (wave >= 2) {
+      #pragma unroll
+      for (int nt = 0; nt < 8; ++nt)
+        #pragma unroll
+        for (int reg = 0; reg < 4; ++reg)
+          cs[(wave-2)*16 + q*4 + reg][nt*16 + l15] = acc[nt][reg] + bv[nt] - lrow[reg];
+    }
+    __syncthreads();
+    #pragma unroll
+    for (int j = 0; j < 4; ++j) {
+      int idx = tid + j*256;
+      int r = idx >> 5, c4 = (idx & 31)*4;
+      int gr = rt*64 + 32 + r;
+      int gc = bn*128 + c4;
+      if (gc + 3 < N) *(float4*)(C + (size_t)gr*N + gc) = *(float4*)&cs[r][c4];
+      else { for (int e = 0; e < 4; ++e) if (gc + e < N) C[(size_t)gr*N + gc + e] = cs[r][c4 + e]; }
     }
   }
 }
 
 __global__ __launch_bounds__(256) void k_lpass2(const short* __restrict__ A16,
-    const short* __restrict__ B16, const float* __restrict__ B32,
-    const float* __restrict__ bias, const float* __restrict__ lse,
-    float* __restrict__ C, int M, int N, int bm_off)
+    const float* __restrict__ B32, const float* __restrict__ bias,
+    const float* __restrict__ lse, float* __restrict__ C, int M, int N, int bm_off)
 {
   __shared__ __align__(16) short As[64][136];
   __shared__ __align__(16) short Bs[128][136];
@@ -881,23 +953,13 @@
     int gr = bm*64 + r; if (gr > M-1) gr = M-1;
     *(bf16x8*)&As[r][e] = *(const bf16x8*)(A16 + (size_t)gr*H + e);
   }
-  if (B16) {
-    #pragma unroll
-    for (int i = 0; i < 8; ++i) {
-      int ch = tid + i*256;
-      int r = ch >> 4, e = (ch & 15)*8;
-      int gn = bn*128 + r; if (gn > N-1) gn = N-1;
-      *(bf16x8*)&Bs[r][e] = *(const bf16x8*)(B16 + (size_t)gn*H + e);
-    }
-  } else {
-    #pragma unroll
-    for (int i = 0; i < 8; ++i) {
-      int ch = tid + i*256;
-      int r = ch >> 4, e = (ch & 15)*8;
-      int gn = bn*128 + r; if (gn > N-1) gn = N-1;
-      const float* src = B32 + (size_t)gn*H + e;
-      *(bf16x8*)&Bs[r][e] = pack8(*(const float4*)src, *(const float4*)(src+4));
-    }
+  #pragma unroll
+  for (int i = 0; i < 8; ++i) {
+    int ch = tid + i*256;
+    int r = ch >> 4, e = (ch & 15)*8;
+    int gn = bn*128 + r; if (gn > N-1) gn = N-1;
+    const float* src = B32 + (size_t)gn*H + e;
+    *(bf16x8*)&Bs[r][e] = pack8(*(const float4*)src, *(const float4*)(src+4));
   }
   __syncthreads();
   f32x4 acc[8];
@@ -991,15 +1053,13 @@
   float* OUT = (float*)d_out;
   size_t oPART  = 0;
   size_t oEMB16 = oPART + (size_t)M*NSL*2;
-  size_t oEMBQ  = oEMB16 + (size_t)V*64;
-  size_t oQGI   = oEMBQ + (size_t)NB*TQ*64;
+  size_t oQGI   = oEMB16 + (size_t)V*64;
   size_t oGIAT  = oQGI  + (size_t)NB*TQ*192;
   size_t oU1    = oGIAT + (size_t)NF*192;
   size_t oGATE  = oU1   + (size_t)NF*H;
   size_t oW16   = oGATE + NF;
   float2* partials = (float2*)(OUT + oPART);
   short* EMB16  = (short*)(OUT + oEMB16);
-  short* EMBQ16 = (short*)(OUT + oEMBQ);
   short* QGIsh  = (short*)(OUT + oQGI);
   short* GIATsh = (short*)(OUT + oGIAT);
   float* U1b    = OUT + oU1;
@@ -1017,16 +1077,16 @@
 
   k_cvtall<<<2632, 256, 0, stream>>>(embed, EMB16, fc_W, FCW16,
                                      ig_Wih, qg_Wih, at_Wih, igW16, V*H);
-  k_gather16<<<NB*TQ/8, 256, 0, stream>>>(EMB16, questions, EMBQ16);
-  k_mgemmX<<<dim3(NB*TQ/64, H3/128), 256, 0, stream>>>(EMBQ16, nullptr, qgW16, qg_bih, QGIsh, NB*TQ, H3);
-  k_facts<<<NF/25, 512, 0, stream>>>(EMB16, igW16, facts, fmask, ig_Whh, ig_bih, ig_bhh, encf, TI);
-  k_recgru2<<<NB/16, 512, 0, stream>>>(QGIsh, qmask, qg_Whh, qg_bhh, qvec, mem, TQ);
-  k_mgemmX<<<dim3(NF/64, H3/128), 256, 0, stream>>>(nullptr, encf, atW16, at_bih, GIATsh, NF, H3);
-  k_gatepre2<<<NF/16, 128, 0, stream>>>(encf, qvec, gate_W1, gate_b1, gate_W2, gate_b2, U1b, GATE);
+  k_mgemmX<<<dim3(NB*TQ/64, H3/128), 256, 0, stream>>>(EMB16, questions, qgW16,
+                                                       qg_bih, QGIsh, NB*TQ, H3);
+  k_factsq<<<264, 512, 0, stream>>>(EMB16, igW16, facts, fmask, ig_Whh, ig_bih, ig_bhh,
+                                    encf, QGIsh, qmask, qg_Whh, qg_bhh, qvec, mem);
+  k_giat_gate0<<<500, 256, 0, stream>>>(encf, atW16, at_bih, GIATsh,
+                                        qvec, gate_W1, gate_b1, gate_W2, gate_b2, U1b, GATE);
   k_episode2<<<NB/16, 512, 0, stream>>>(GIATsh, GATE, at_Whh, at_bhh,
                                         me_Wih, me_Whh, me_bih, me_bhh, mem);
   for (int e = 1; e < EPISODES; ++e) {
-    k_gate<<<NF/16, 128, 0, stream>>>(encf, mem, gate_W1, gate_W2, gate_b2, U1b, GATE);
+    k_gate256<<<NF/32, 256, 0, stream>>>(encf, mem, gate_W1, gate_W2, gate_b2, U1b, GATE);
     k_episode2<<<NB/16, 512, 0, stream>>>(GIATsh, GATE, at_Whh, at_bhh,
                                           me_Wih, me_Whh, me_bih, me_bhh, mem);
   }
@@ -1035,6 +1095,6 @@
   k_lpass1p<<<NSL, 256, 0, stream>>>(H2D16, FCW16, fc_b, partials, M, V, NSL);
   k_lse2<<<(M+3)/4, 256, 0, stream>>>(partials, lse, M, NSL);
   k_lpass2p<<<NSL, 256, 0, stream>>>(H2D16, FCW16, fc_b, lse, OUT, M, V, (M/64) - 1);
-  k_lpass2<<<dim3(1, NSL), 256, 0, stream>>>(H2D16, nullptr, fc_W, fc_b, lse,
+  k_lpass2<<<dim3(1, NSL), 256, 0, stream>>>(H2D16, fc_W, fc_b, lse,
                                              OUT, M, V, (M/64) - 1);
 }
```

New measurement: 921.5 us. 1.04x faster.
